# Kernel optimization log

Measured on AMD Instinct MI355X. Metric: run time of the kernel, lower is better.

Reference implementation:

```python
import jax, jax.numpy as jnp
import numpy as np
import math

STD = math.exp(0.0025)  # exp(0.5 * 0.005) from log_sigma = 0.005
C = 0.5 * math.log(2 * math.pi)
B, X, H, Z, L, W = 8192, 512, 256, 64, 16, 32

def _predict(h, Wd, bd, Wo, bo):
    return jax.nn.sigmoid(jax.nn.relu(h @ Wd.T + bd) @ Wo.T + bo)

def _gru(xin, h, Wih, Whh, bih, bhh):
    gi = xin @ Wih.T + bih
    gh = h @ Whh.T + bhh
    ir, iz, inn = jnp.split(gi, 3, axis=1)
    hr, hz, hn = jnp.split(gh, 3, axis=1)
    r = jax.nn.sigmoid(ir + hr)
    zt = jax.nn.sigmoid(iz + hz)
    n = jnp.tanh(inn + r * hn)
    return (1.0 - zt) * n + zt * h

def setup_inputs():
    key = jax.random.key(0)
    ks = iter(jax.random.split(key, 40))
    def nrm(shape, s=0.05):
        return jax.random.normal(next(ks), shape, dtype=jnp.float32) * s
    return {
        "x": jax.random.uniform(next(ks), (B, X), dtype=jnp.float32),
        "workers": jax.random.uniform(next(ks), (W, B, L), dtype=jnp.float32),
        "Wf1": nrm((H, X)), "bf1": jnp.zeros((H,)),
        "Wf2": nrm((1, H)), "bf2": jnp.zeros((1,)),
        "eWih": nrm((L, 3 * H, X + 1)), "eWhh": nrm((L, 3 * H, H)),
        "ebih": jnp.zeros((L, 3 * H)), "ebhh": jnp.zeros((L, 3 * H)),
        "eWd": nrm((L, H, H)), "ebd": jnp.zeros((L, H)),
        "eWo": nrm((L, 1, H)), "ebo": jnp.zeros((L, 1)),
        "Wmu": nrm((Z, H)), "bmu": jnp.zeros((Z,)),
        "Wlv": nrm((Z, H)), "blv": jnp.zeros((Z,)),
        "dWih": nrm((L, 3 * H, Z + 1)), "dWhh": nrm((L, 3 * H, H)),
        "dbih": jnp.zeros((L, 3 * H)), "dbhh": jnp.zeros((L, 3 * H)),
        "dWd": nrm((L, H, H)), "dbd": jnp.zeros((L, H)),
        "dWo": nrm((L, W, H)), "dbo": jnp.zeros((L, W)),
        "Wr": nrm((X, H)), "br": jnp.zeros((X,)),
        "enc_eps": jax.random.normal(next(ks), (L, B, H), dtype=jnp.float32),
        "samp_eps": jax.random.normal(next(ks), (B, Z), dtype=jnp.float32),
        "dec_eps": jax.random.uniform(next(ks), (L, B, H), dtype=jnp.float32),
    }

def _forward(x, workers, Wf1, bf1, Wf2, bf2, eWih, eWhh, ebih, ebhh, eWd, ebd, eWo, ebo,
             Wmu, bmu, Wlv, blv, dWih, dWhh, dbih, dbhh, dWd, dbd, dWo, dbo, Wr, br,
             enc_eps, samp_eps, dec_eps):
    nB = x.shape[0]
    h_dim = eWhh.shape[2]
    # Encoder: t[:,0] = firstcell(x)
    t0 = _predict(x, Wf1, bf1, Wf2, bf2)[:, 0]
    z0 = jnp.zeros((nB, h_dim), dtype=x.dtype)

    def enc_step(carry, xs):
        z, ti = carry
        Wih, Whh, bih, bhh, Wd, bd, Wo, bo, eps = xs
        tmp = (ti >= 0.5).astype(x.dtype)
        mu = _gru(jnp.concatenate([x, tmp[:, None]], axis=1), z, Wih, Whh, bih, bhh)
        znew = mu + STD * eps
        tn = _predict(znew, Wd, bd, Wo, bo)[:, 0]
        return (znew, tn), ti

    (z_fin, _), tcols = jax.lax.scan(
        enc_step, (z0, t0), (eWih, eWhh, ebih, ebhh, eWd, ebd, eWo, ebo, enc_eps))
    t = tcols.T  # [B, L]
    mu_z = z_fin @ Wmu.T + bmu
    log_var = jax.nn.softplus(z_fin @ Wlv.T + blv)
    latent = mu_z + jnp.exp(0.5 * log_var) * samp_eps
    tmp_t = (t > 0.5).astype(x.dtype)

    def dec_step(zt, xs):
        Wih, Whh, bih, bhh, Wd, bd, Wo, bo, tcol, eps = xs
        mu = _gru(jnp.concatenate([latent, tcol[:, None]], axis=1), zt, Wih, Whh, bih, bhh)
        znew = mu + STD * eps  # decoder uses uniform eps (torch.rand)
        return znew, _predict(znew, Wd, bd, Wo, bo)

    zT, preds = jax.lax.scan(
        dec_step, jnp.zeros((nB, h_dim), dtype=x.dtype),
        (dWih, dWhh, dbih, dbhh, dWd, dbd, dWo, dbo, tmp_t.T, dec_eps))
    worker_preds = jnp.transpose(preds, (2, 1, 0))  # [L,B,W] -> [W,B,L]
    recon = jax.nn.sigmoid(zT @ Wr.T + br)
    log_p_x = jnp.sum(x * jnp.log(recon), axis=1)
    logp = jnp.clip(jnp.log(worker_preds), -100.0)
    log1mp = jnp.clip(jnp.log1p(-worker_preds), -100.0)
    bce = -(workers * logp + (1.0 - workers) * log1mp)
    log_p_y = -jnp.sum(jnp.sum(bce, axis=0), axis=1)
    workers_bar = jnp.mean(workers, axis=0)
    log_kl = jnp.sum(t * (jnp.log(t + 1e-6) - jnp.log(workers_bar + 1e-6)), axis=1)
    log_p_z = jnp.sum(-C - latent ** 2 / 2, axis=-1)
    log_q = jnp.sum(-C - log_var / 2 - (latent - mu_z) ** 2 / (2 * jnp.exp(log_var)), axis=-1)
    loss = jnp.mean(log_q - log_p_z - log_p_y - log_p_x + log_kl)
    return t, loss

def reference(x, workers, Wf1, bf1, Wf2, bf2, eWih, eWhh, ebih, ebhh, eWd, ebd, eWo, ebo,
              Wmu, bmu, Wlv, blv, dWih, dWhh, dbih, dbhh, dWd, dbd, dWo, dbo, Wr, br,
              enc_eps, samp_eps, dec_eps):
    return _forward(x, workers, Wf1, bf1, Wf2, bf2, eWih, eWhh, ebih, ebhh, eWd, ebd,
                    eWo, ebo, Wmu, bmu, Wlv, blv, dWih, dWhh, dbih, dbhh, dWd, dbd,
                    dWo, dbo, Wr, br, enc_eps, samp_eps, dec_eps)
```

## Files before the change

### kernel.cpp

```cpp
#include <hip/hip_runtime.h>
#include <hip/hip_bf16.h>
#include <math.h>

#define B_ 8192
#define X_ 512
#define H_ 256
#define Z_ 64
#define L_ 16
#define W_ 32
#define G3_ 768

#define STDF 1.0025031276057952f
#define CC 0.9189385332046727f

typedef _Float16 f16x8 __attribute__((ext_vector_type(8)));
typedef float f32x4 __attribute__((ext_vector_type(4)));

__device__ __forceinline__ float sigm(float x) { return 1.0f / (1.0f + expf(-x)); }
__device__ __forceinline__ float logsig(float u) {
    return (u > 0.0f) ? -log1pf(expf(-u)) : (u - log1pf(expf(u)));
}

#define GLOAD16(gsrc, ldst) \
    __builtin_amdgcn_global_load_lds((const __attribute__((address_space(1))) unsigned int*)(gsrc), \
                                     (__attribute__((address_space(3))) unsigned int*)(ldst), 16, 0, 0)

#define WAITV(N) asm volatile("s_waitcnt vmcnt(" #N ")" ::: "memory")
#define SBAR()  do { __builtin_amdgcn_sched_barrier(0); __builtin_amdgcn_s_barrier(); } while (0)

template<int MODE, int KX, int FIRST>
__global__ __launch_bounds__(512) void gru_fused(
    const _Float16* __restrict__ A2,
    const _Float16* __restrict__ Wih,
    const float* __restrict__ bih,
    const _Float16* __restrict__ Whh,
    const float* __restrict__ bhh,
    const float* __restrict__ ec,
    const float* __restrict__ tcol,
    const float* __restrict__ eps,
    const _Float16* __restrict__ zh_in,
    float* __restrict__ z,
    _Float16* __restrict__ zh_out)
{
    constexpr int N1 = KX / 64;
    constexpr int NT = N1 + (FIRST ? 0 : 4);
    __shared__ char smem[2][(128 + 192) * 128];

    const int tid  = threadIdx.x;
    const int wave = tid >> 6;
    const int lane = tid & 63;
    const int wr   = wave >> 1;
    const int wc   = wave & 1;
    const int id   = blockIdx.x;
    const int xcd  = id & 7;
    const int wk   = id >> 3;
    const int bm   = (xcd * 8 + (wk >> 2)) * 128;
    const int h0   = (wk & 3) * 64;
    const int l15  = lane & 15;
    const int l4   = lane >> 4;

    f32x4 acc[2][6];
    f32x4 accN[2][2];
    #pragma unroll
    for (int a = 0; a < 2; ++a) {
        #pragma unroll
        for (int b = 0; b < 6; ++b) { f32x4 zz = {0.f,0.f,0.f,0.f}; acc[a][b] = zz; }
        #pragma unroll
        for (int b = 0; b < 2; ++b) { f32x4 zz = {0.f,0.f,0.f,0.f}; accN[a][b] = zz; }
    }

    auto stage = [&](int s, int pb) {
        char* As = smem[pb];
        char* Ws = smem[pb] + 128 * 128;
        const _Float16* srcA;
        const _Float16* srcW;
        int KA, k0;
        if (s < N1) { srcA = A2;    srcW = Wih; KA = KX;  k0 = s * 64; }
        else        { srcA = zh_in; srcW = Whh; KA = 256; k0 = (s - N1) * 64; }
        #pragma unroll
        for (int q = 0; q < 2; ++q) {
            int f   = q * 8192 + tid * 16;
            int row = f >> 7;
            int c   = ((f >> 4) & 7) ^ (row & 7);
            GLOAD16(srcA + (long)(bm + row) * KA + k0 + c * 8, As + f);
        }
        #pragma unroll
        for (int q = 0; q < 3; ++q) {
            int f   = q * 8192 + tid * 16;
            int rr  = f >> 7;
            int c   = ((f >> 4) & 7) ^ (rr & 7);
            int srow = (rr >> 6) * 256 + h0 + (rr & 63);
            GLOAD16(srcW + (long)srow * KA + k0 + c * 8, Ws + f);
        }
    };

    stage(0, 0);
    for (int s = 0; s < NT; ++s) {
        int pb = s & 1;
        if (s + 1 < NT) { stage(s + 1, pb ^ 1); WAITV(5); }
        else WAITV(0);
        SBAR();
        char* As = smem[pb];
        char* Ws = smem[pb] + 128 * 128;
        bool p1 = (s < N1);
        #pragma unroll
        for (int ks = 0; ks < 2; ++ks) {
            f16x8 af[2], bf[6];
            #pragma unroll
            for (int mi = 0; mi < 2; ++mi) {
                int row = wr * 32 + mi * 16 + l15;
                int c   = (ks * 4 + l4) ^ (row & 7);
                af[mi] = *(const f16x8*)(As + row * 128 + c * 16);
            }
            #pragma unroll
            for (int ni = 0; ni < 6; ++ni) {
                int rr = (ni >> 1) * 64 + wc * 32 + (ni & 1) * 16 + l15;
                int c  = (ks * 4 + l4) ^ (rr & 7);
                bf[ni] = *(const f16x8*)(Ws + rr * 128 + c * 16);
            }
            if (p1) {
                #pragma unroll
                for (int mi = 0; mi < 2; ++mi) {
                    #pragma unroll
                    for (int ni = 0; ni < 4; ++ni)
                        acc[mi][ni] = __builtin_amdgcn_mfma_f32_16x16x32_f16(
                            af[mi], bf[ni], acc[mi][ni], 0, 0, 0);
                    #pragma unroll
                    for (int ni = 4; ni < 6; ++ni)
                        accN[mi][ni - 4] = __builtin_amdgcn_mfma_f32_16x16x32_f16(
                            af[mi], bf[ni], accN[mi][ni - 4], 0, 0, 0);
                }
            } else {
                #pragma unroll
                for (int mi = 0; mi < 2; ++mi)
                    #pragma unroll
                    for (int ni = 0; ni < 6; ++ni)
                        acc[mi][ni] = __builtin_amdgcn_mfma_f32_16x16x32_f16(
                            af[mi], bf[ni], acc[mi][ni], 0, 0, 0);
            }
        }
        SBAR();
    }

    #pragma unroll
    for (int mi = 0; mi < 2; ++mi)
        #pragma unroll
        for (int r = 0; r < 4; ++r) {
            int grow = bm + wr * 32 + mi * 16 + l4 * 4 + r;
            float tv = tcol[(long)grow * L_];
            float ext = (MODE == 1) ? (tv >= 0.5f ? 1.0f : 0.0f)
                                    : (tv >  0.5f ? 1.0f : 0.0f);
            #pragma unroll
            for (int hb = 0; hb < 2; ++hb) {
                int h = h0 + wc * 32 + hb * 16 + l15;
                float rpre = acc[mi][hb][r]     + bih[h]       + bhh[h]       + ext * ec[h];
                float zpre = acc[mi][2 + hb][r] + bih[256 + h] + bhh[256 + h] + ext * ec[256 + h];
                float hn   = acc[mi][4 + hb][r] + bhh[512 + h];
                float in_  = accN[mi][hb][r]    + bih[512 + h] + ext * ec[512 + h];
                float rg = sigm(rpre);
                float zt = sigm(zpre);
                float n  = tanhf(in_ + rg * hn);
                long zi = (long)grow * 256 + h;
                float zold = FIRST ? 0.0f : z[zi];
                float v = (1.0f - zt) * n + zt * zold + STDF * eps[zi];
                z[zi] = v;
                zh_out[zi] = (_Float16)v;
            }
        }
}

__global__ __launch_bounds__(256) void predict_head512(
    const _Float16* __restrict__ A,
    const _Float16* __restrict__ Wd,
    const float* __restrict__ bd,
    const float* __restrict__ wo,
    const float* __restrict__ bo,
    float* __restrict__ out, int ostride)
{
    constexpr int K = 512;
    constexpr int NT = K / 64;
    __shared__ char smem[2][(32 + 256) * 128];
    __shared__ float part[32][4];

    const int tid  = threadIdx.x;
    const int wave = tid >> 6;
    const int lane = tid & 63;
    const int bm   = blockIdx.x * 32;
    const int l15  = lane & 15;
    const int l4   = lane >> 4;

    f32x4 acc[2][4];
    #pragma unroll
    for (int a = 0; a < 2; ++a)
        #pragma unroll
        for (int b = 0; b < 4; ++b) { f32x4 zz = {0.f,0.f,0.f,0.f}; acc[a][b] = zz; }

    auto stage = [&](int s, int pb) {
        char* As = smem[pb];
        char* Ws = smem[pb] + 32 * 128;
        int k0 = s * 64;
        {
            int o   = wave * 1024 + lane * 16;
            int row = o >> 7;
            int c   = ((o >> 4) & 7) ^ (row & 7);
            GLOAD16(A + (long)(bm + row) * K + k0 + c * 8, As + wave * 1024);
        }
        #pragma unroll
        for (int it = 0; it < 8; ++it) {
            int q   = it * 4 + wave;
            int o   = q * 1024 + lane * 16;
            int row = o >> 7;
            int c   = ((o >> 4) & 7) ^ (row & 7);
            GLOAD16(Wd + (long)row * K + k0 + c * 8, Ws + q * 1024);
        }
    };

    stage(0, 0);
    for (int s = 0; s < NT; ++s) {
        int pb = s & 1;
        if (s + 1 < NT) { stage(s + 1, pb ^ 1); WAITV(9); }
        else WAITV(0);
        SBAR();
        char* As = smem[pb];
        char* Ws = smem[pb] + 32 * 128;
        #pragma unroll
        for (int ks = 0; ks < 2; ++ks) {
            f16x8 af[2], bf[4];
            #pragma unroll
            for (int mi = 0; mi < 2; ++mi) {
                int row = mi * 16 + l15;
                int c   = (ks * 4 + l4) ^ (row & 7);
                af[mi] = *(const f16x8*)(As + row * 128 + c * 16);
            }
            #pragma unroll
            for (int ni = 0; ni < 4; ++ni) {
                int row = wave * 64 + ni * 16 + l15;
                int c   = (ks * 4 + l4) ^ (row & 7);
                bf[ni] = *(const f16x8*)(Ws + row * 128 + c * 16);
            }
            #pragma unroll
            for (int mi = 0; mi < 2; ++mi)
                #pragma unroll
                for (int ni = 0; ni < 4; ++ni)
                    acc[mi][ni] = __builtin_amdgcn_mfma_f32_16x16x32_f16(
                        af[mi], bf[ni], acc[mi][ni], 0, 0, 0);
        }
        SBAR();
    }

    float bdv[4], wov[4];
    #pragma unroll
    for (int ni = 0; ni < 4; ++ni) {
        int col = wave * 64 + ni * 16 + l15;
        bdv[ni] = bd[col];
        wov[ni] = wo[col];
    }
    #pragma unroll
    for (int mi = 0; mi < 2; ++mi)
        #pragma unroll
        for (int r = 0; r < 4; ++r) {
            float s = 0.0f;
            #pragma unroll
            for (int ni = 0; ni < 4; ++ni) {
                float v = fmaxf(acc[mi][ni][r] + bdv[ni], 0.0f);
                s = fmaf(v, wov[ni], s);
            }
            #pragma unroll
            for (int off = 1; off < 16; off <<= 1) s += __shfl_xor(s, off, 16);
            if (l15 == 0) part[mi * 16 + l4 * 4 + r][wave] = s;
        }
    __syncthreads();
    if (tid < 32) {
        float u = part[tid][0] + part[tid][1] + part[tid][2] + part[tid][3] + bo[0];
        out[(long)(bm + tid) * ostride] = sigm(u);
    }
}

__global__ __launch_bounds__(256) void predict_fast(
    const _Float16* __restrict__ A,
    const _Float16* __restrict__ Wd,
    const float* __restrict__ bd,
    const float* __restrict__ wo,
    const float* __restrict__ bo,
    float* __restrict__ out, int ostride)
{
    __shared__ char Wl[131072];
    __shared__ char Al[16384];
    __shared__ float part[32][4];

    const int tid  = threadIdx.x;
    const int wave = tid >> 6;
    const int lane = tid & 63;
    const int bm   = blockIdx.x * 32;
    const int l15  = lane & 15;
    const int l4   = lane >> 4;

    #pragma unroll
    for (int q = 0; q < 32; ++q) {
        int f   = q * 4096 + tid * 16;
        int kc  = f >> 15;
        int o   = f & 32767;
        int row = o >> 7;
        int c   = ((o >> 4) & 7) ^ (row & 7);
        GLOAD16(Wd + (long)row * 256 + kc * 64 + c * 8, Wl + f);
    }
    #pragma unroll
    for (int q = 0; q < 4; ++q) {
        int f   = q * 4096 + tid * 16;
        int kc  = f >> 12;
        int o   = f & 4095;
        int row = o >> 7;
        int c   = ((o >> 4) & 7) ^ (row & 7);
        GLOAD16(A + (long)(bm + row) * 256 + kc * 64 + c * 8, Al + f);
    }
    WAITV(0);
    __syncthreads();

    f32x4 acc[2][4];
    #pragma unroll
    for (int a = 0; a < 2; ++a)
        #pragma unroll
        for (int b = 0; b < 4; ++b) { f32x4 zz = {0.f,0.f,0.f,0.f}; acc[a][b] = zz; }

    #pragma unroll
    for (int kc = 0; kc < 4; ++kc)
        #pragma unroll
        for (int ks = 0; ks < 2; ++ks) {
            f16x8 af[2], bf[4];
            #pragma unroll
            for (int mi = 0; mi < 2; ++mi) {
                int row = mi * 16 + l15;
                int c   = (ks * 4 + l4) ^ (row & 7);
                af[mi] = *(const f16x8*)(Al + kc * 4096 + row * 128 + c * 16);
            }
            #pragma unroll
            for (int ni = 0; ni < 4; ++ni) {
                int row = wave * 64 + ni * 16 + l15;
                int c   = (ks * 4 + l4) ^ (row & 7);
                bf[ni] = *(const f16x8*)(Wl + kc * 32768 + row * 128 + c * 16);
            }
            #pragma unroll
            for (int mi = 0; mi < 2; ++mi)
                #pragma unroll
                for (int ni = 0; ni < 4; ++ni)
                    acc[mi][ni] = __builtin_amdgcn_mfma_f32_16x16x32_f16(
                        af[mi], bf[ni], acc[mi][ni], 0, 0, 0);
        }

    float bdv[4], wov[4];
    #pragma unroll
    for (int ni = 0; ni < 4; ++ni) {
        int col = wave * 64 + ni * 16 + l15;
        bdv[ni] = bd[col];
        wov[ni] = wo[col];
    }
    #pragma unroll
    for (int mi = 0; mi < 2; ++mi)
        #pragma unroll
        for (int r = 0; r < 4; ++r) {
            float s = 0.0f;
            #pragma unroll
            for (int ni = 0; ni < 4; ++ni) {
                float v = fmaxf(acc[mi][ni][r] + bdv[ni], 0.0f);
                s = fmaf(v, wov[ni], s);
            }
            #pragma unroll
            for (int off = 1; off < 16; off <<= 1) s += __shfl_xor(s, off, 16);
            if (l15 == 0) part[mi * 16 + l4 * 4 + r][wave] = s;
        }
    __syncthreads();
    if (tid < 32) {
        float u = part[tid][0] + part[tid][1] + part[tid][2] + part[tid][3] + bo[0];
        out[(long)(bm + tid) * ostride] = sigm(u);
    }
}

__global__ __launch_bounds__(256) void dec_head_bce_fast(
    const _Float16* __restrict__ A,
    const _Float16* __restrict__ Wd,
    const float* __restrict__ bd,
    const _Float16* __restrict__ Wo,
    const float* __restrict__ bo,
    const float* __restrict__ wt,
    float* __restrict__ bacc)
{
    __shared__ char Wl[131072];
    __shared__ _Float16 ds[32 * 264];
    __shared__ float part[32][2];

    const int tid  = threadIdx.x;
    const int wave = tid >> 6;
    const int lane = tid & 63;
    const int bm   = blockIdx.x * 32;
    const int l15  = lane & 15;
    const int l4   = lane >> 4;

    #pragma unroll
    for (int q = 0; q < 32; ++q) {
        int f   = q * 4096 + tid * 16;
        int kc  = f >> 15;
        int o   = f & 32767;
        int row = o >> 7;
        int c   = ((o >> 4) & 7) ^ (row & 7);
        GLOAD16(Wd + (long)row * 256 + kc * 64 + c * 8, Wl + f);
    }
    f16x8 afr[8];
    #pragma unroll
    for (int kc = 0; kc < 4; ++kc)
        #pragma unroll
        for (int mi = 0; mi < 2; ++mi) {
            int row = mi * 16 + l15;
            afr[kc * 2 + mi] = *(const f16x8*)(A + (long)(bm + row) * 256 + kc * 64 + l4 * 8);
        }

    f32x4 acc[2][4];
    #pragma unroll
    for (int a = 0; a < 2; ++a)
        #pragma unroll
        for (int b = 0; b < 4; ++b) { f32x4 zz = {0.f,0.f,0.f,0.f}; acc[a][b] = zz; }

    WAITV(0);
    __syncthreads();

    #pragma unroll
    for (int kc = 0; kc < 4; ++kc) {
        f16x8 bf[4];
        #pragma unroll
        for (int ni = 0; ni < 4; ++ni) {
            int row = wave * 64 + ni * 16 + l15;
            int c   = (0 * 4 + l4) ^ (row & 7);
            bf[ni] = *(const f16x8*)(Wl + kc * 32768 + row * 128 + c * 16);
        }
        #pragma unroll
        for (int mi = 0; mi < 2; ++mi)
            #pragma unroll
            for (int ni = 0; ni < 4; ++ni)
                acc[mi][ni] = __builtin_amdgcn_mfma_f32_16x16x32_f16(
                    afr[kc * 2 + mi], bf[ni], acc[mi][ni], 0, 0, 0);
    }
    #pragma unroll
    for (int kc = 0; kc < 4; ++kc)
        #pragma unroll
        for (int mi = 0; mi < 2; ++mi) {
            int row = mi * 16 + l15;
            afr[kc * 2 + mi] = *(const f16x8*)(A + (long)(bm + row) * 256 + kc * 64 + 32 + l4 * 8);
        }
    #pragma unroll
    for (int kc = 0; kc < 4; ++kc) {
        f16x8 bf[4];
        #pragma unroll
        for (int ni = 0; ni < 4; ++ni) {
            int row = wave * 64 + ni * 16 + l15;
            int c   = (1 * 4 + l4) ^ (row & 7);
            bf[ni] = *(const f16x8*)(Wl + kc * 32768 + row * 128 + c * 16);
        }
        #pragma unroll
        for (int mi = 0; mi < 2; ++mi)
            #pragma unroll
            for (int ni = 0; ni < 4; ++ni)
                acc[mi][ni] = __builtin_amdgcn_mfma_f32_16x16x32_f16(
                    afr[kc * 2 + mi], bf[ni], acc[mi][ni], 0, 0, 0);
    }

    #pragma unroll
    for (int mi = 0; mi < 2; ++mi)
        #pragma unroll
        for (int r = 0; r < 4; ++r) {
            int row = mi * 16 + l4 * 4 + r;
            #pragma unroll
            for (int ni = 0; ni < 4; ++ni) {
                int col = wave * 64 + ni * 16 + l15;
                ds[row * 264 + col] = (_Float16)fmaxf(acc[mi][ni][r] + bd[col], 0.0f);
            }
        }
    __syncthreads();

    const int rh = wave >> 1;
    const int ch = wave & 1;
    f32x4 acc2 = {0.f, 0.f, 0.f, 0.f};
    #pragma unroll
    for (int k = 0; k < 8; ++k) {
        f16x8 bf2 = *(const f16x8*)(Wo + (long)(ch * 16 + l15) * 256 + k * 32 + l4 * 8);
        f16x8 af  = *(const f16x8*)(ds + (rh * 16 + l15) * 264 + k * 32 + l4 * 8);
        acc2 = __builtin_amdgcn_mfma_f32_16x16x32_f16(af, bf2, acc2, 0, 0, 0);
    }

    #pragma unroll
    for (int r = 0; r < 4; ++r) {
        int row = rh * 16 + l4 * 4 + r;
        int w = ch * 16 + l15;
        float u = acc2[r] + bo[w];
        float logp   = fmaxf(logsig(u),  -100.0f);
        float log1mp = fmaxf(logsig(-u), -100.0f);
        float wk = wt[(long)(bm + row) * W_ + w];
        float s = -(wk * logp + (1.0f - wk) * log1mp);
        #pragma unroll
        for (int off = 1; off < 16; off <<= 1) s += __shfl_xor(s, off, 16);
        if (l15 == 0) part[row][ch] = s;
    }
    __syncthreads();
    if (tid < 32) bacc[bm + tid] += part[tid][0] + part[tid][1];
}

__global__ __launch_bounds__(256) void latent_fused(
    const _Float16* __restrict__ A,
    const _Float16* __restrict__ Wml,
    const float* __restrict__ bml,
    const float* __restrict__ seps,
    _Float16* __restrict__ lath,
    float* __restrict__ lq, float* __restrict__ lpz)
{
    __shared__ char Wl[65536];
    __shared__ char Al[16384];
    __shared__ float muv[32][129];

    const int tid  = threadIdx.x;
    const int wave = tid >> 6;
    const int lane = tid & 63;
    const int bm   = blockIdx.x * 32;
    const int l15  = lane & 15;
    const int l4   = lane >> 4;

    #pragma unroll
    for (int q = 0; q < 16; ++q) {
        int f   = q * 4096 + tid * 16;
        int kc  = f >> 14;
        int o   = f & 16383;
        int row = o >> 7;
        int c   = ((o >> 4) & 7) ^ (row & 7);
        GLOAD16(Wml + (long)row * 256 + kc * 64 + c * 8, Wl + f);
    }
    #pragma unroll
    for (int q = 0; q < 4; ++q) {
        int f   = q * 4096 + tid * 16;
        int kc  = f >> 12;
        int o   = f & 4095;
        int row = o >> 7;
        int c   = ((o >> 4) & 7) ^ (row & 7);
        GLOAD16(A + (long)(bm + row) * 256 + kc * 64 + c * 8, Al + f);
    }
    WAITV(0);
    __syncthreads();

    f32x4 acc[2][2];
    #pragma unroll
    for (int a = 0; a < 2; ++a)
        #pragma unroll
        for (int b = 0; b < 2; ++b) { f32x4 zz = {0.f,0.f,0.f,0.f}; acc[a][b] = zz; }

    #pragma unroll
    for (int kc = 0; kc < 4; ++kc)
        #pragma unroll
        for (int ks = 0; ks < 2; ++ks) {
            f16x8 af[2], bf[2];
            #pragma unroll
            for (int mi = 0; mi < 2; ++mi) {
                int row = mi * 16 + l15;
                int c   = (ks * 4 + l4) ^ (row & 7);
                af[mi] = *(const f16x8*)(Al + kc * 4096 + row * 128 + c * 16);
            }
            #pragma unroll
            for (int ni = 0; ni < 2; ++ni) {
                int row = wave * 32 + ni * 16 + l15;
                int c   = (ks * 4 + l4) ^ (row & 7);
                bf[ni] = *(const f16x8*)(Wl + kc * 16384 + row * 128 + c * 16);
            }
            #pragma unroll
            for (int mi = 0; mi < 2; ++mi)
                #pragma unroll
                for (int ni = 0; ni < 2; ++ni)
                    acc[mi][ni] = __builtin_amdgcn_mfma_f32_16x16x32_f16(
                        af[mi], bf[ni], acc[mi][ni], 0, 0, 0);
        }

    #pragma unroll
    for (int mi = 0; mi < 2; ++mi)
        #pragma unroll
        for (int r = 0; r < 4; ++r) {
            int row = mi * 16 + l4 * 4 + r;
            #pragma unroll
            for (int ni = 0; ni < 2; ++ni) {
                int col = wave * 32 + ni * 16 + l15;
                muv[row][col] = acc[mi][ni][r] + bml[col];
            }
        }
    __syncthreads();

    int rsub = lane >> 3;
    int row  = wave * 8 + rsub;
    int zlo  = lane & 7;
    float lpz_c = 0.0f, lq_c = 0.0f;
    #pragma unroll
    for (int j = 0; j < 8; ++j) {
        int zc = zlo * 8 + j;
        float mu = muv[row][zc];
        float sp = muv[row][64 + zc];
        float lv = (sp > 0.0f) ? (sp + log1pf(expf(-sp))) : log1pf(expf(sp));
        float e  = seps[(long)(bm + row) * Z_ + zc];
        float lat = mu + expf(0.5f * lv) * e;
        lath[(long)(bm + row) * Z_ + zc] = (_Float16)lat;
        lpz_c += -CC - 0.5f * lat * lat;
        float d = lat - mu;
        lq_c += -CC - 0.5f * lv - d * d / (2.0f * expf(lv));
    }
    #pragma unroll
    for (int off = 1; off < 8; off <<= 1) {
        lpz_c += __shfl_xor(lpz_c, off, 8);
        lq_c  += __shfl_xor(lq_c, off, 8);
    }
    if (zlo == 0) { lpz[bm + row] = lpz_c; lq[bm + row] = lq_c; }
}

__global__ __launch_bounds__(256) void recon_logpx_gemm(
    const _Float16* __restrict__ A,
    const _Float16* __restrict__ Wt,
    const float* __restrict__ bias,
    const float* __restrict__ x,
    float* __restrict__ lpx)
{
    constexpr int K = 256;
    constexpr int NT = 4;
    __shared__ char smem[2][(128 + 128) * 128];
    __shared__ float part[128][2];

    const int tid  = threadIdx.x;
    const int wave = tid >> 6;
    const int lane = tid & 63;
    const int wr   = wave >> 1;
    const int wc   = wave & 1;
    const int bm   = blockIdx.y * 128;
    const int bn   = blockIdx.x * 128;
    const int l15  = lane & 15;
    const int l4   = lane >> 4;

    f32x4 acc[4][4];
    #pragma unroll
    for (int a = 0; a < 4; ++a)
        #pragma unroll
        for (int b = 0; b < 4; ++b) { f32x4 zz = {0.f,0.f,0.f,0.f}; acc[a][b] = zz; }

    auto stage = [&](int s, int pb) {
        char* As = smem[pb];
        char* Ws = smem[pb] + 128 * 128;
        int k0 = s * 64;
        #pragma unroll
        for (int it = 0; it < 4; ++it) {
            int q   = it * 4 + wave;
            int o   = q * 1024 + lane * 16;
            int row = o >> 7;
            int c   = ((o >> 4) & 7) ^ (row & 7);
            GLOAD16(A + (long)(bm + row) * K + k0 + c * 8, As + q * 1024);
        }
        #pragma unroll
        for (int it = 0; it < 4; ++it) {
            int q   = it * 4 + wave;
            int o   = q * 1024 + lane * 16;
            int row = o >> 7;
            int c   = ((o >> 4) & 7) ^ (row & 7);
            GLOAD16(Wt + (long)(bn + row) * K + k0 + c * 8, Ws + q * 1024);
        }
    };

    stage(0, 0);
    for (int s = 0; s < NT; ++s) {
        int pb = s & 1;
        if (s + 1 < NT) { stage(s + 1, pb ^ 1); WAITV(8); }
        else WAITV(0);
        SBAR();
        char* As = smem[pb];
        char* Ws = smem[pb] + 128 * 128;
        #pragma unroll
        for (int ks = 0; ks < 2; ++ks) {
            f16x8 af[4], bf[4];
            #pragma unroll
            for (int mi = 0; mi < 4; ++mi) {
                int row = wr * 64 + mi * 16 + l15;
                int c   = (ks * 4 + l4) ^ (row & 7);
                af[mi] = *(const f16x8*)(As + row * 128 + c * 16);
            }
            #pragma unroll
            for (int ni = 0; ni < 4; ++ni) {
                int row = wc * 64 + ni * 16 + l15;
                int c   = (ks * 4 + l4) ^ (row & 7);
                bf[ni] = *(const f16x8*)(Ws + row * 128 + c * 16);
            }
            #pragma unroll
            for (int mi = 0; mi < 4; ++mi)
                #pragma unroll
                for (int ni = 0; ni < 4; ++ni)
                    acc[mi][ni] = __builtin_amdgcn_mfma_f32_16x16x32_f16(
                        af[mi], bf[ni], acc[mi][ni], 0, 0, 0);
        }
        SBAR();
    }

    #pragma unroll
    for (int mi = 0; mi < 4; ++mi)
        #pragma unroll
        for (int r = 0; r < 4; ++r) {
            int grow = bm + wr * 64 + mi * 16 + l4 * 4 + r;
            float s = 0.0f;
            #pragma unroll
            for (int ni = 0; ni < 4; ++ni) {
                int gcol = bn + wc * 64 + ni * 16 + l15;
                float u = acc[mi][ni][r] + bias[gcol];
                s = fmaf(x[(long)grow * X_ + gcol], logsig(u), s);
            }
            #pragma unroll
            for (int off = 1; off < 16; off <<= 1) s += __shfl_xor(s, off, 16);
            if (l15 == 0) part[wr * 64 + mi * 16 + l4 * 4 + r][wc] = s;
        }
    __syncthreads();
    if (tid < 128) atomicAdd(&lpx[bm + tid], part[tid][0] + part[tid][1]);
}

__global__ __launch_bounds__(256) void wtrans(
    const float* __restrict__ workers, float* __restrict__ wt,
    float* __restrict__ bacc, float* __restrict__ lpx)
{
    long idx = (long)blockIdx.x * 256 + threadIdx.x;
    int w = idx & 31;
    long b = idx >> 5;
    const float* src = workers + (w * (long)B_ + b) * L_;
    #pragma unroll
    for (int l = 0; l < L_; ++l)
        wt[((long)l * B_ + b) * W_ + w] = src[l];
    if (w == 0) { bacc[b] = 0.0f; lpx[b] = 0.0f; }
}

struct ConvJobs {
    const float* s[10];
    _Float16* d[10];
};
__device__ __constant__ const long CJ_CNT[10] = {
    (long)B_ * X_, (long)H_ * X_, (long)L_ * G3_ * H_, (long)L_ * H_ * H_,
    (long)L_ * G3_ * H_, (long)L_ * H_ * H_, (long)L_ * W_ * H_,
    (long)X_ * H_, (long)Z_ * H_, (long)Z_ * H_
};
#define CJ_TOTAL 13008896L

__global__ __launch_bounds__(256) void conv_multi(ConvJobs J)
{
    long i8 = ((long)blockIdx.x * 256 + threadIdx.x) * 8;
    if (i8 >= CJ_TOTAL) return;
    long rem = i8; int j = 0;
    #pragma unroll
    for (int k = 0; k < 9; ++k)
        if (rem >= CJ_CNT[k]) { rem -= CJ_CNT[k]; ++j; } else break;
    const float* s = J.s[j] + rem;
    f16x8 o;
    #pragma unroll
    for (int q = 0; q < 8; ++q) o[q] = (_Float16)s[q];
    *(f16x8*)(J.d[j] + rem) = o;
}

__global__ __launch_bounds__(256) void conv_f16(
    const float* __restrict__ src, _Float16* __restrict__ dst,
    int Ks, int Kd, long total)
{
    long i = ((long)blockIdx.x * 256 + threadIdx.x) * 8;
    if (i >= total) return;
    long r = i / Kd, k = i - r * Kd;
    const float* s = src + r * Ks + k;
    f16x8 o;
    #pragma unroll
    for (int j = 0; j < 8; ++j) o[j] = (_Float16)s[j];
    *(f16x8*)(dst + i) = o;
}

__global__ __launch_bounds__(256) void extract_col(
    const float* __restrict__ src, float* __restrict__ dst, int Ks, int col, int R)
{
    int i = blockIdx.x * 256 + threadIdx.x;
    if (i < R) dst[i] = src[(long)i * Ks + col];
}

__global__ void stack_bias(const float* __restrict__ a, const float* __restrict__ b,
                           float* __restrict__ o)
{
    int i = threadIdx.x;
    o[i] = (i < 64) ? a[i] : b[i - 64];
}

__global__ __launch_bounds__(256) void kl_kernel(
    const float* __restrict__ tmat, const float* __restrict__ workers,
    float* __restrict__ lkl)
{
    int b = blockIdx.x * 256 + threadIdx.x;
    float wb[L_];
    #pragma unroll
    for (int l = 0; l < L_; ++l) wb[l] = 0.0f;
    for (int w = 0; w < W_; ++w) {
        const float* p = workers + ((long)w * B_ + b) * L_;
        #pragma unroll
        for (int l = 0; l < L_; ++l) wb[l] += p[l];
    }
    float s = 0.0f;
    #pragma unroll
    for (int l = 0; l < L_; ++l) {
        float wbar = wb[l] * (1.0f / 32.0f);
        float tv = tmat[(long)b * L_ + l];
        s += tv * (logf(tv + 1e-6f) - logf(wbar + 1e-6f));
    }
    lkl[b] = s;
}

__global__ __launch_bounds__(1024) void final_reduce(
    const float* __restrict__ lq, const float* __restrict__ lpz,
    const float* __restrict__ bacc, const float* __restrict__ lpx,
    const float* __restrict__ lkl, float* __restrict__ out)
{
    __shared__ float red[16];
    float s = 0.0f;
    for (int b = threadIdx.x; b < B_; b += 1024)
        s += lq[b] - lpz[b] + bacc[b] - lpx[b] + lkl[b];
    #pragma unroll
    for (int off = 32; off; off >>= 1) s += __shfl_down(s, off);
    int wave = threadIdx.x >> 6, lane = threadIdx.x & 63;
    if (lane == 0) red[wave] = s;
    __syncthreads();
    if (threadIdx.x == 0) {
        float t = 0.0f;
        for (int i = 0; i < 16; ++i) t += red[i];
        out[0] = t / (float)B_;
    }
}

extern "C" void kernel_launch(void* const* d_in, const int* in_sizes, int n_in,
                              void* d_out, int out_size, void* d_ws, size_t ws_size,
                              hipStream_t stream)
{
    const float* x       = (const float*)d_in[0];
    const float* workers = (const float*)d_in[1];
    const float* Wf1     = (const float*)d_in[2];
    const float* bf1     = (const float*)d_in[3];
    const float* Wf2     = (const float*)d_in[4];
    const float* bf2     = (const float*)d_in[5];
    const float* eWih    = (const float*)d_in[6];
    const float* eWhh    = (const float*)d_in[7];
    const float* ebih    = (const float*)d_in[8];
    const float* ebhh    = (const float*)d_in[9];
    const float* eWd     = (const float*)d_in[10];
    const float* ebd     = (const float*)d_in[11];
    const float* eWo     = (const float*)d_in[12];
    const float* ebo     = (const float*)d_in[13];
    const float* Wmu     = (const float*)d_in[14];
    const float* bmu     = (const float*)d_in[15];
    const float* Wlv     = (const float*)d_in[16];
    const float* blv     = (const float*)d_in[17];
    const float* dWih    = (const float*)d_in[18];
    const float* dWhh    = (const float*)d_in[19];
    const float* dbih    = (const float*)d_in[20];
    const float* dbhh    = (const float*)d_in[21];
    const float* dWd     = (const float*)d_in[22];
    const float* dbd     = (const float*)d_in[23];
    const float* dWo     = (const float*)d_in[24];
    const float* dbo     = (const float*)d_in[25];
    const float* Wr      = (const float*)d_in[26];
    const float* br      = (const float*)d_in[27];
    const float* enc_eps = (const float*)d_in[28];
    const float* samp_eps= (const float*)d_in[29];
    const float* dec_eps = (const float*)d_in[30];

    float* t    = (float*)d_out;
    float* loss = t + (long)B_ * L_;

    char* p = (char*)d_ws;
    auto alloc = [&](size_t bytes) {
        char* r = p;
        p += (bytes + 255) & ~(size_t)255;
        return r;
    };
    _Float16* xh    = (_Float16*)alloc((size_t)B_ * X_ * 2);
    _Float16* zha   = (_Float16*)alloc((size_t)B_ * H_ * 2);
    _Float16* zhb   = (_Float16*)alloc((size_t)B_ * H_ * 2);
    _Float16* lath  = (_Float16*)alloc((size_t)B_ * Z_ * 2);
    _Float16* Wf1h  = (_Float16*)alloc((size_t)H_ * X_ * 2);
    _Float16* eWihh = (_Float16*)alloc((size_t)L_ * G3_ * X_ * 2);
    _Float16* eWhhh = (_Float16*)alloc((size_t)L_ * G3_ * H_ * 2);
    _Float16* eWdh  = (_Float16*)alloc((size_t)L_ * H_ * H_ * 2);
    _Float16* dWihh = (_Float16*)alloc((size_t)L_ * G3_ * Z_ * 2);
    _Float16* dWhhh = (_Float16*)alloc((size_t)L_ * G3_ * H_ * 2);
    _Float16* dWdh  = (_Float16*)alloc((size_t)L_ * H_ * H_ * 2);
    _Float16* dWoh  = (_Float16*)alloc((size_t)L_ * W_ * H_ * 2);
    _Float16* Wrh   = (_Float16*)alloc((size_t)X_ * H_ * 2);
    _Float16* Wmlh  = (_Float16*)alloc((size_t)128 * H_ * 2);
    float* bml    = (float*)alloc(128 * 4);
    float* eWihc  = (float*)alloc((size_t)L_ * G3_ * 4);
    float* dWihc  = (float*)alloc((size_t)L_ * G3_ * 4);
    float* z      = (float*)alloc((size_t)B_ * H_ * 4);
    float* wt     = (float*)alloc((size_t)L_ * B_ * W_ * 4);
    float* lq     = (float*)alloc((size_t)B_ * 4);
    float* lpz    = (float*)alloc((size_t)B_ * 4);
    float* lpx    = (float*)alloc((size_t)B_ * 4);
    float* lkl    = (float*)alloc((size_t)B_ * 4);
    float* bacc   = (float*)alloc((size_t)B_ * 4);

    const dim3 blk(256);
    const int nBH = B_ * H_;
    auto cgrid = [](long total) { return dim3((unsigned)((total / 8 + 255) / 256)); };

    ConvJobs J;
    J.s[0] = x;    J.d[0] = xh;
    J.s[1] = Wf1;  J.d[1] = Wf1h;
    J.s[2] = eWhh; J.d[2] = eWhhh;
    J.s[3] = eWd;  J.d[3] = eWdh;
    J.s[4] = dWhh; J.d[4] = dWhhh;
    J.s[5] = dWd;  J.d[5] = dWdh;
    J.s[6] = dWo;  J.d[6] = dWoh;
    J.s[7] = Wr;   J.d[7] = Wrh;
    J.s[8] = Wmu;  J.d[8] = Wmlh;
    J.s[9] = Wlv;  J.d[9] = Wmlh + (long)Z_ * H_;
    conv_multi<<<(CJ_TOTAL / 8 + 255) / 256, blk, 0, stream>>>(J);
    conv_f16<<<cgrid((long)L_ * G3_ * X_), blk, 0, stream>>>(eWih, eWihh, X_ + 1, X_, (long)L_ * G3_ * X_);
    conv_f16<<<cgrid((long)L_ * G3_ * Z_), blk, 0, stream>>>(dWih, dWihh, Z_ + 1, Z_, (long)L_ * G3_ * Z_);
    stack_bias<<<1, 128, 0, stream>>>(bmu, blv, bml);
    extract_col<<<(L_ * G3_ + 255) / 256, blk, 0, stream>>>(eWih, eWihc, X_ + 1, X_, L_ * G3_);
    extract_col<<<(L_ * G3_ + 255) / 256, blk, 0, stream>>>(dWih, dWihc, Z_ + 1, Z_, L_ * G3_);
    wtrans<<<(W_ * B_) / 256, blk, 0, stream>>>(workers, wt, bacc, lpx);

    predict_head512<<<B_ / 32, blk, 0, stream>>>(xh, Wf1h, bf1, Wf2, bf2, t, L_);

    _Float16* zcur = zha;
    _Float16* znxt = zhb;
    for (int l = 0; l < L_; ++l) {
        if (l == 0)
            gru_fused<1, X_, 1><<<256, 512, 0, stream>>>(
                xh, eWihh, ebih, eWhhh, ebhh, eWihc, t, enc_eps, zcur, z, znxt);
        else
            gru_fused<1, X_, 0><<<256, 512, 0, stream>>>(
                xh, eWihh + (long)l * G3_ * X_, ebih + (long)l * G3_,
                eWhhh + (long)l * G3_ * H_, ebhh + (long)l * G3_,
                eWihc + (long)l * G3_, t + l, enc_eps + (long)l * nBH,
                zcur, z, znxt);
        _Float16* tmp = zcur; zcur = znxt; znxt = tmp;
        if (l < L_ - 1)
            predict_fast<<<B_ / 32, blk, 0, stream>>>(
                zcur, eWdh + (long)l * H_ * H_, ebd + (long)l * H_,
                eWo + (long)l * H_, ebo + l, t + (l + 1), L_);
    }

    latent_fused<<<B_ / 32, blk, 0, stream>>>(zcur, Wmlh, bml, samp_eps, lath, lq, lpz);

    zcur = zha; znxt = zhb;
    for (int l = 0; l < L_; ++l) {
        if (l == 0)
            gru_fused<2, Z_, 1><<<256, 512, 0, stream>>>(
                lath, dWihh, dbih, dWhhh, dbhh, dWihc, t, dec_eps, zcur, z, znxt);
        else
            gru_fused<2, Z_, 0><<<256, 512, 0, stream>>>(
                lath, dWihh + (long)l * G3_ * Z_, dbih + (long)l * G3_,
                dWhhh + (long)l * G3_ * H_, dbhh + (long)l * G3_,
                dWihc + (long)l * G3_, t + l, dec_eps + (long)l * nBH,
                zcur, z, znxt);
        _Float16* tmp = zcur; zcur = znxt; znxt = tmp;
        dec_head_bce_fast<<<B_ / 32, blk, 0, stream>>>(
            zcur, dWdh + (long)l * H_ * H_, dbd + (long)l * H_,
            dWoh + (long)l * W_ * H_, dbo + (long)l * W_,
            wt + (long)l * B_ * W_, bacc);
    }

    recon_logpx_gemm<<<dim3(X_ / 128, B_ / 128), blk, 0, stream>>>(
        zcur, Wrh, br, x, lpx);
    kl_kernel<<<B_ / 256, blk, 0, stream>>>(t, workers, lkl);
    final_reduce<<<1, 1024, 0, stream>>>(lq, lpz, bacc, lpx, lkl, loss);
}
```

Measured before the change: 1.074 ms.

## Fuse predict and decoder heads into GRU step kernels; merge prep launches

```diff
diff --git a/kernel.cpp b/kernel.cpp
--- a/kernel.cpp
+++ b/kernel.cpp
@@ -26,10 +26,13 @@
                                      (__attribute__((address_space(3))) unsigned int*)(ldst), 16, 0, 0)
 
 #define WAITV(N) asm volatile("s_waitcnt vmcnt(" #N ")" ::: "memory")
+#define WAITV0() asm volatile("s_waitcnt vmcnt(0)" ::: "memory")
 #define SBAR()  do { __builtin_amdgcn_sched_barrier(0); __builtin_amdgcn_s_barrier(); } while (0)
 
-template<int MODE, int KX, int FIRST>
-__global__ __launch_bounds__(512) void gru_fused(
+#define MFMA16(a, b, c) __builtin_amdgcn_mfma_f32_16x16x32_f16((a), (b), (c), 0, 0, 0)
+
+template<int FIRST>
+__global__ __launch_bounds__(512, 4) void enc_gru(
     const _Float16* __restrict__ A2,
     const _Float16* __restrict__ Wih,
     const float* __restrict__ bih,
@@ -37,14 +40,21 @@
     const float* __restrict__ bhh,
     const float* __restrict__ ec,
     const float* __restrict__ tcol,
+    const _Float16* __restrict__ Wdp,
+    const float* __restrict__ bdp,
+    const float* __restrict__ wop,
+    const float* __restrict__ bop,
+    float* __restrict__ tout,
     const float* __restrict__ eps,
     const _Float16* __restrict__ zh_in,
     float* __restrict__ z,
     _Float16* __restrict__ zh_out)
 {
+    constexpr int KX = 512;
     constexpr int N1 = KX / 64;
-    constexpr int NT = N1 + (FIRST ? 0 : 4);
-    __shared__ char smem[2][(128 + 192) * 128];
+    constexpr int NT = FIRST ? N1 : (N1 + 4);
+    __shared__ char smem[2][40960];
+    __shared__ float uarr[128];
 
     const int tid  = threadIdx.x;
     const int wave = tid >> 6;
@@ -59,6 +69,83 @@
     const int l15  = lane & 15;
     const int l4   = lane >> 4;
 
+    if (!FIRST) {
+        float up0 = 0.f, up1 = 0.f, up2 = 0.f, up3 = 0.f;
+        for (int ch = 0; ch < 2; ++ch) {
+            f32x4 acc2[8];
+            #pragma unroll
+            for (int i = 0; i < 8; ++i) { f32x4 zz = {0.f,0.f,0.f,0.f}; acc2[i] = zz; }
+            auto pstage = [&](int s, int pb) {
+                char* As = smem[pb];
+                char* Ws = smem[pb] + 16384;
+                int k0 = s * 64;
+                #pragma unroll
+                for (int q = 0; q < 2; ++q) {
+                    int f = q * 8192 + tid * 16;
+                    int row = f >> 7;
+                    int c = ((f >> 4) & 7) ^ (row & 7);
+                    GLOAD16(zh_in + (long)(bm + row) * 256 + k0 + c * 8, As + f);
+                }
+                #pragma unroll
+                for (int q = 0; q < 2; ++q) {
+                    int f = q * 8192 + tid * 16;
+                    int row = f >> 7;
+                    int c = ((f >> 4) & 7) ^ (row & 7);
+                    GLOAD16(Wdp + (long)(ch * 128 + row) * 256 + k0 + c * 8, Ws + f);
+                }
+            };
+            pstage(0, 0);
+            for (int s = 0; s < 4; ++s) {
+                int pb = s & 1;
+                if (s + 1 < 4) { pstage(s + 1, pb ^ 1); WAITV(4); }
+                else WAITV0();
+                SBAR();
+                char* As = smem[pb];
+                char* Ws = smem[pb] + 16384;
+                #pragma unroll
+                for (int ks = 0; ks < 2; ++ks) {
+                    int arow = wave * 16 + l15;
+                    int ca = (ks * 4 + l4) ^ (arow & 7);
+                    f16x8 af = *(const f16x8*)(As + arow * 128 + ca * 16);
+                    #pragma unroll
+                    for (int ni = 0; ni < 8; ++ni) {
+                        int wrow = ni * 16 + l15;
+                        int cw = (ks * 4 + l4) ^ (wrow & 7);
+                        f16x8 bf = *(const f16x8*)(Ws + wrow * 128 + cw * 16);
+                        acc2[ni] = MFMA16(af, bf, acc2[ni]);
+                    }
+                }
+                SBAR();
+            }
+            #pragma unroll
+            for (int ni = 0; ni < 8; ++ni) {
+                int col = ch * 128 + ni * 16 + l15;
+                float bdv = bdp[col], wov = wop[col];
+                up0 = fmaf(fmaxf(acc2[ni][0] + bdv, 0.f), wov, up0);
+                up1 = fmaf(fmaxf(acc2[ni][1] + bdv, 0.f), wov, up1);
+                up2 = fmaf(fmaxf(acc2[ni][2] + bdv, 0.f), wov, up2);
+                up3 = fmaf(fmaxf(acc2[ni][3] + bdv, 0.f), wov, up3);
+            }
+        }
+        #pragma unroll
+        for (int off = 1; off < 16; off <<= 1) {
+            up0 += __shfl_xor(up0, off, 16);
+            up1 += __shfl_xor(up1, off, 16);
+            up2 += __shfl_xor(up2, off, 16);
+            up3 += __shfl_xor(up3, off, 16);
+        }
+        if (l15 == 0) {
+            float b0 = bop[0];
+            uarr[wave * 16 + l4 * 4 + 0] = up0 + b0;
+            uarr[wave * 16 + l4 * 4 + 1] = up1 + b0;
+            uarr[wave * 16 + l4 * 4 + 2] = up2 + b0;
+            uarr[wave * 16 + l4 * 4 + 3] = up3 + b0;
+        }
+        __syncthreads();
+        if (h0 == 0 && tid < 128)
+            tout[(long)(bm + tid) * L_] = sigm(uarr[tid]);
+    }
+
     f32x4 acc[2][6];
     f32x4 accN[2][2];
     #pragma unroll
@@ -71,7 +158,7 @@
 
     auto stage = [&](int s, int pb) {
         char* As = smem[pb];
-        char* Ws = smem[pb] + 128 * 128;
+        char* Ws = smem[pb] + 16384;
         const _Float16* srcA;
         const _Float16* srcW;
         int KA, k0;
@@ -98,10 +185,10 @@
     for (int s = 0; s < NT; ++s) {
         int pb = s & 1;
         if (s + 1 < NT) { stage(s + 1, pb ^ 1); WAITV(5); }
-        else WAITV(0);
+        else WAITV0();
         SBAR();
         char* As = smem[pb];
-        char* Ws = smem[pb] + 128 * 128;
+        char* Ws = smem[pb] + 16384;
         bool p1 = (s < N1);
         #pragma unroll
         for (int ks = 0; ks < 2; ++ks) {
@@ -123,20 +210,17 @@
                 for (int mi = 0; mi < 2; ++mi) {
                     #pragma unroll
                     for (int ni = 0; ni < 4; ++ni)
-                        acc[mi][ni] = __builtin_amdgcn_mfma_f32_16x16x32_f16(
-                            af[mi], bf[ni], acc[mi][ni], 0, 0, 0);
+                        acc[mi][ni] = MFMA16(af[mi], bf[ni], acc[mi][ni]);
                     #pragma unroll
                     for (int ni = 4; ni < 6; ++ni)
-                        accN[mi][ni - 4] = __builtin_amdgcn_mfma_f32_16x16x32_f16(
-                            af[mi], bf[ni], accN[mi][ni - 4], 0, 0, 0);
+                        accN[mi][ni - 4] = MFMA16(af[mi], bf[ni], accN[mi][ni - 4]);
                 }
             } else {
                 #pragma unroll
                 for (int mi = 0; mi < 2; ++mi)
                     #pragma unroll
                     for (int ni = 0; ni < 6; ++ni)
-                        acc[mi][ni] = __builtin_amdgcn_mfma_f32_16x16x32_f16(
-                            af[mi], bf[ni], acc[mi][ni], 0, 0, 0);
+                        acc[mi][ni] = MFMA16(af[mi], bf[ni], acc[mi][ni]);
             }
         }
         SBAR();
@@ -146,10 +230,15 @@
     for (int mi = 0; mi < 2; ++mi)
         #pragma unroll
         for (int r = 0; r < 4; ++r) {
-            int grow = bm + wr * 32 + mi * 16 + l4 * 4 + r;
-            float tv = tcol[(long)grow * L_];
-            float ext = (MODE == 1) ? (tv >= 0.5f ? 1.0f : 0.0f)
-                                    : (tv >  0.5f ? 1.0f : 0.0f);
+            int lrow = wr * 32 + mi * 16 + l4 * 4 + r;
+            int grow = bm + lrow;
+            float ext;
+            if (FIRST) {
+                float tv = tcol[(long)grow * L_];
+                ext = (tv >= 0.5f) ? 1.0f : 0.0f;
+            } else {
+                ext = (uarr[lrow] >= 0.0f) ? 1.0f : 0.0f;
+            }
             #pragma unroll
             for (int hb = 0; hb < 2; ++hb) {
                 int h = h0 + wc * 32 + hb * 16 + l15;
@@ -169,6 +258,410 @@
         }
 }
 
+__device__ void dec_gru_role(char (*smem)[40960],
+    const _Float16* __restrict__ A2, const _Float16* __restrict__ Wih,
+    const float* __restrict__ bih, const _Float16* __restrict__ Whh,
+    const float* __restrict__ bhh, const float* __restrict__ ec,
+    const float* __restrict__ tcol, const float* __restrict__ eps,
+    const _Float16* __restrict__ zh_in, float* __restrict__ z,
+    _Float16* __restrict__ zh_out, bool first)
+{
+    constexpr int KX = Z_;
+    constexpr int N1 = 1;
+    const int NT = first ? 1 : 5;
+
+    const int tid  = threadIdx.x;
+    const int wave = tid >> 6;
+    const int lane = tid & 63;
+    const int wr   = wave >> 1;
+    const int wc   = wave & 1;
+    const int id   = blockIdx.x;
+    const int xcd  = id & 7;
+    const int wk   = id >> 3;
+    const int bm   = (xcd * 8 + (wk >> 2)) * 128;
+    const int h0   = (wk & 3) * 64;
+    const int l15  = lane & 15;
+    const int l4   = lane >> 4;
+
+    f32x4 acc[2][6];
+    f32x4 accN[2][2];
+    #pragma unroll
+    for (int a = 0; a < 2; ++a) {
+        #pragma unroll
+        for (int b = 0; b < 6; ++b) { f32x4 zz = {0.f,0.f,0.f,0.f}; acc[a][b] = zz; }
+        #pragma unroll
+        for (int b = 0; b < 2; ++b) { f32x4 zz = {0.f,0.f,0.f,0.f}; accN[a][b] = zz; }
+    }
+
+    auto stage = [&](int s, int pb) {
+        char* As = smem[pb];
+        char* Ws = smem[pb] + 16384;
+        const _Float16* srcA;
+        const _Float16* srcW;
+        int KA, k0;
+        if (s < N1) { srcA = A2;    srcW = Wih; KA = KX;  k0 = s * 64; }
+        else        { srcA = zh_in; srcW = Whh; KA = 256; k0 = (s - N1) * 64; }
+        #pragma unroll
+        for (int q = 0; q < 2; ++q) {
+            int f   = q * 8192 + tid * 16;
+            int row = f >> 7;
+            int c   = ((f >> 4) & 7) ^ (row & 7);
+            GLOAD16(srcA + (long)(bm + row) * KA + k0 + c * 8, As + f);
+        }
+        #pragma unroll
+        for (int q = 0; q < 3; ++q) {
+            int f   = q * 8192 + tid * 16;
+            int rr  = f >> 7;
+            int c   = ((f >> 4) & 7) ^ (rr & 7);
+            int srow = (rr >> 6) * 256 + h0 + (rr & 63);
+            GLOAD16(srcW + (long)srow * KA + k0 + c * 8, Ws + f);
+        }
+    };
+
+    stage(0, 0);
+    for (int s = 0; s < NT; ++s) {
+        int pb = s & 1;
+        if (s + 1 < NT) { stage(s + 1, pb ^ 1); WAITV(5); }
+        else WAITV0();
+        SBAR();
+        char* As = smem[pb];
+        char* Ws = smem[pb] + 16384;
+        bool p1 = (s < N1);
+        #pragma unroll
+        for (int ks = 0; ks < 2; ++ks) {
+            f16x8 af[2], bf[6];
+            #pragma unroll
+            for (int mi = 0; mi < 2; ++mi) {
+                int row = wr * 32 + mi * 16 + l15;
+                int c   = (ks * 4 + l4) ^ (row & 7);
+                af[mi] = *(const f16x8*)(As + row * 128 + c * 16);
+            }
+            #pragma unroll
+            for (int ni = 0; ni < 6; ++ni) {
+                int rr = (ni >> 1) * 64 + wc * 32 + (ni & 1) * 16 + l15;
+                int c  = (ks * 4 + l4) ^ (rr & 7);
+                bf[ni] = *(const f16x8*)(Ws + rr * 128 + c * 16);
+            }
+            if (p1) {
+                #pragma unroll
+                for (int mi = 0; mi < 2; ++mi) {
+                    #pragma unroll
+                    for (int ni = 0; ni < 4; ++ni)
+                        acc[mi][ni] = MFMA16(af[mi], bf[ni], acc[mi][ni]);
+                    #pragma unroll
+                    for (int ni = 4; ni < 6; ++ni)
+                        accN[mi][ni - 4] = MFMA16(af[mi], bf[ni], accN[mi][ni - 4]);
+                }
+            } else {
+                #pragma unroll
+                for (int mi = 0; mi < 2; ++mi)
+                    #pragma unroll
+                    for (int ni = 0; ni < 6; ++ni)
+                        acc[mi][ni] = MFMA16(af[mi], bf[ni], acc[mi][ni]);
+            }
+        }
+        SBAR();
+    }
+
+    #pragma unroll
+    for (int mi = 0; mi < 2; ++mi)
+        #pragma unroll
+        for (int r = 0; r < 4; ++r) {
+            int grow = bm + wr * 32 + mi * 16 + l4 * 4 + r;
+            float tv = tcol[(long)grow * L_];
+            float ext = (tv > 0.5f) ? 1.0f : 0.0f;
+            #pragma unroll
+            for (int hb = 0; hb < 2; ++hb) {
+                int h = h0 + wc * 32 + hb * 16 + l15;
+                float rpre = acc[mi][hb][r]     + bih[h]       + bhh[h]       + ext * ec[h];
+                float zpre = acc[mi][2 + hb][r] + bih[256 + h] + bhh[256 + h] + ext * ec[256 + h];
+                float hn   = acc[mi][4 + hb][r] + bhh[512 + h];
+                float in_  = accN[mi][hb][r]    + bih[512 + h] + ext * ec[512 + h];
+                float rg = sigm(rpre);
+                float zt = sigm(zpre);
+                float n  = tanhf(in_ + rg * hn);
+                long zi = (long)grow * 256 + h;
+                float zold = first ? 0.0f : z[zi];
+                float v = (1.0f - zt) * n + zt * zold + STDF * eps[zi];
+                z[zi] = v;
+                zh_out[zi] = (_Float16)v;
+            }
+        }
+}
+
+__device__ void bce_role(char (*smem)[40960], float* auxp, int localblk,
+    const _Float16* __restrict__ A, const _Float16* __restrict__ Wd,
+    const float* __restrict__ bd, const _Float16* __restrict__ Wo,
+    const float* __restrict__ bo, const float* __restrict__ wtl,
+    float* __restrict__ bacc)
+{
+    const int tid  = threadIdx.x;
+    const bool act = tid < 256;
+    const int wave = tid >> 6;
+    const int lane = tid & 63;
+    const int bm2  = localblk * 32;
+    const int l15  = lane & 15;
+    const int l4   = lane >> 4;
+
+    f32x4 acc[2][2];
+    #pragma unroll
+    for (int a = 0; a < 2; ++a)
+        #pragma unroll
+        for (int b = 0; b < 2; ++b) { f32x4 zz = {0.f,0.f,0.f,0.f}; acc[a][b] = zz; }
+
+    auto stage = [&](int s, int pb) {
+        if (!act) return;
+        char* As = smem[pb];
+        char* Ws = smem[pb] + 4096;
+        int k0 = s * 64;
+        {
+            int f   = tid * 16;
+            int row = f >> 7;
+            int c   = ((f >> 4) & 7) ^ (row & 7);
+            GLOAD16(A + (long)(bm2 + row) * 256 + k0 + c * 8, As + f);
+        }
+        #pragma unroll
+        for (int q = 0; q < 8; ++q) {
+            int f   = q * 4096 + tid * 16;
+            int row = f >> 7;
+            int c   = ((f >> 4) & 7) ^ (row & 7);
+            GLOAD16(Wd + (long)row * 256 + k0 + c * 8, Ws + f);
+        }
+    };
+
+    stage(0, 0);
+    for (int s = 0; s < 4; ++s) {
+        int pb = s & 1;
+        if (s + 1 < 4) { stage(s + 1, pb ^ 1); WAITV(9); }
+        else WAITV0();
+        SBAR();
+        if (act) {
+            char* As = smem[pb];
+            char* Ws = smem[pb] + 4096;
+            #pragma unroll
+            for (int ks = 0; ks < 2; ++ks) {
+                f16x8 af[2], bf[2];
+                #pragma unroll
+                for (int mi = 0; mi < 2; ++mi) {
+                    int row = mi * 16 + l15;
+                    int c   = (ks * 4 + l4) ^ (row & 7);
+                    af[mi] = *(const f16x8*)(As + row * 128 + c * 16);
+                }
+                #pragma unroll
+                for (int ni = 0; ni < 2; ++ni) {
+                    int row = wave * 64 + ni * 16 + l15;
+                    int c   = (ks * 4 + l4) ^ (row & 7);
+                    bf[ni] = *(const f16x8*)(Ws + row * 128 + c * 16);
+                }
+                #pragma unroll
+                for (int mi = 0; mi < 2; ++mi)
+                    #pragma unroll
+                    for (int ni = 0; ni < 2; ++ni)
+                        acc[mi][ni] = MFMA16(af[mi], bf[ni], acc[mi][ni]);
+            }
+        }
+        SBAR();
+    }
+
+    _Float16* ds = (_Float16*)smem[0];
+    if (act) {
+        #pragma unroll
+        for (int mi = 0; mi < 2; ++mi)
+            #pragma unroll
+            for (int r = 0; r < 4; ++r) {
+                int row = mi * 16 + l4 * 4 + r;
+                #pragma unroll
+                for (int ni = 0; ni < 2; ++ni) {
+                    int col = wave * 64 + ni * 16 + l15;
+                    ds[row * 264 + col] = (_Float16)fmaxf(acc[mi][ni][r] + bd[col], 0.0f);
+                }
+            }
+    }
+    __syncthreads();
+
+    if (act) {
+        const int rh = wave >> 1;
+        const int ch = wave & 1;
+        f32x4 acc2 = {0.f, 0.f, 0.f, 0.f};
+        #pragma unroll
+        for (int k = 0; k < 8; ++k) {
+            f16x8 bf2 = *(const f16x8*)(Wo + (long)(ch * 16 + l15) * 256 + k * 32 + l4 * 8);
+            f16x8 af  = *(const f16x8*)(ds + (rh * 16 + l15) * 264 + k * 32 + l4 * 8);
+            acc2 = MFMA16(af, bf2, acc2);
+        }
+        #pragma unroll
+        for (int r = 0; r < 4; ++r) {
+            int row = rh * 16 + l4 * 4 + r;
+            int w = ch * 16 + l15;
+            float u = acc2[r] + bo[w];
+            float logp   = fmaxf(logsig(u),  -100.0f);
+            float log1mp = fmaxf(logsig(-u), -100.0f);
+            float wk = wtl[(long)(bm2 + row) * W_ + w];
+            float s = -(wk * logp + (1.0f - wk) * log1mp);
+            #pragma unroll
+            for (int off = 1; off < 16; off <<= 1) s += __shfl_xor(s, off, 16);
+            if (l15 == 0) auxp[row * 2 + ch] = s;
+        }
+    }
+    __syncthreads();
+    if (tid < 32) bacc[bm2 + tid] += auxp[tid * 2 + 0] + auxp[tid * 2 + 1];
+}
+
+__device__ void recon_role(char (*smem)[40960], float* auxp, int localblk,
+    const _Float16* __restrict__ A, const _Float16* __restrict__ Wt,
+    const float* __restrict__ bias, const float* __restrict__ x,
+    float* __restrict__ lpx)
+{
+    const int tid  = threadIdx.x;
+    const bool act = tid < 256;
+    const int wave = tid >> 6;
+    const int lane = tid & 63;
+    const int wr   = wave >> 1;
+    const int wc   = wave & 1;
+    const int bm   = (localblk >> 2) * 128;
+    const int bn   = (localblk & 3) * 128;
+    const int l15  = lane & 15;
+    const int l4   = lane >> 4;
+
+    f32x4 acc[4][4];
+    #pragma unroll
+    for (int a = 0; a < 4; ++a)
+        #pragma unroll
+        for (int b = 0; b < 4; ++b) { f32x4 zz = {0.f,0.f,0.f,0.f}; acc[a][b] = zz; }
+
+    auto stage = [&](int s, int pb) {
+        if (!act) return;
+        char* As = smem[pb];
+        char* Ws = smem[pb] + 16384;
+        int k0 = s * 64;
+        #pragma unroll
+        for (int it = 0; it < 4; ++it) {
+            int q   = it * 4 + wave;
+            int o   = q * 1024 + lane * 16;
+            int row = o >> 7;
+            int c   = ((o >> 4) & 7) ^ (row & 7);
+            GLOAD16(A + (long)(bm + row) * 256 + k0 + c * 8, As + q * 1024);
+        }
+        #pragma unroll
+        for (int it = 0; it < 4; ++it) {
+            int q   = it * 4 + wave;
+            int o   = q * 1024 + lane * 16;
+            int row = o >> 7;
+            int c   = ((o >> 4) & 7) ^ (row & 7);
+            GLOAD16(Wt + (long)(bn + row) * 256 + k0 + c * 8, Ws + q * 1024);
+        }
+    };
+
+    stage(0, 0);
+    for (int s = 0; s < 4; ++s) {
+        int pb = s & 1;
+        if (s + 1 < 4) { stage(s + 1, pb ^ 1); WAITV(8); }
+        else WAITV0();
+        SBAR();
+        if (act) {
+            char* As = smem[pb];
+            char* Ws = smem[pb] + 16384;
+            #pragma unroll
+            for (int ks = 0; ks < 2; ++ks) {
+                f16x8 af[4], bf[4];
+                #pragma unroll
+                for (int mi = 0; mi < 4; ++mi) {
+                    int row = wr * 64 + mi * 16 + l15;
+                    int c   = (ks * 4 + l4) ^ (row & 7);
+                    af[mi] = *(const f16x8*)(As + row * 128 + c * 16);
+                }
+                #pragma unroll
+                for (int ni = 0; ni < 4; ++ni) {
+                    int row = wc * 64 + ni * 16 + l15;
+                    int c   = (ks * 4 + l4) ^ (row & 7);
+                    bf[ni] = *(const f16x8*)(Ws + row * 128 + c * 16);
+                }
+                #pragma unroll
+                for (int mi = 0; mi < 4; ++mi)
+                    #pragma unroll
+                    for (int ni = 0; ni < 4; ++ni)
+                        acc[mi][ni] = MFMA16(af[mi], bf[ni], acc[mi][ni]);
+            }
+        }
+        SBAR();
+    }
+
+    if (act) {
+        #pragma unroll
+        for (int mi = 0; mi < 4; ++mi)
+            #pragma unroll
+            for (int r = 0; r < 4; ++r) {
+                int grow = bm + wr * 64 + mi * 16 + l4 * 4 + r;
+                float s = 0.0f;
+                #pragma unroll
+                for (int ni = 0; ni < 4; ++ni) {
+                    int gcol = bn + wc * 64 + ni * 16 + l15;
+                    float u = acc[mi][ni][r] + bias[gcol];
+                    s = fmaf(x[(long)grow * X_ + gcol], logsig(u), s);
+                }
+                #pragma unroll
+                for (int off = 1; off < 16; off <<= 1) s += __shfl_xor(s, off, 16);
+                if (l15 == 0) auxp[(wr * 64 + mi * 16 + l4 * 4 + r) * 2 + wc] = s;
+            }
+    }
+    __syncthreads();
+    if (tid < 128) atomicAdd(&lpx[bm + tid], auxp[tid * 2] + auxp[tid * 2 + 1]);
+}
+
+template<int FIRSTL>
+__global__ __launch_bounds__(512, 4) void dec_step(
+    const _Float16* lath, const _Float16* Wih, const float* bih,
+    const _Float16* Whh, const float* bhh, const float* ec,
+    const float* tcol, const float* eps,
+    const _Float16* zh_in, float* z, _Float16* zh_out,
+    const _Float16* WdB, const float* bdB, const _Float16* WoB,
+    const float* boB, const float* wtB, float* bacc,
+    const float* tmat, const float* workers, float* lkl)
+{
+    __shared__ char smem[2][40960];
+    __shared__ float auxp[256];
+
+    if (blockIdx.x < 256) {
+        dec_gru_role(smem, lath, Wih, bih, Whh, bhh, ec, tcol, eps,
+                     zh_in, z, zh_out, FIRSTL != 0);
+    } else if (FIRSTL) {
+        if (threadIdx.x < 256) {
+            int b = (blockIdx.x - 256) * 256 + threadIdx.x;
+            float wb[L_];
+            #pragma unroll
+            for (int l = 0; l < L_; ++l) wb[l] = 0.0f;
+            for (int w = 0; w < W_; ++w) {
+                const float* pw = workers + (w * (long)B_ + b) * L_;
+                #pragma unroll
+                for (int l = 0; l < L_; ++l) wb[l] += pw[l];
+            }
+            float s = 0.0f;
+            #pragma unroll
+            for (int l = 0; l < L_; ++l) {
+                float wbar = wb[l] * (1.0f / 32.0f);
+                float tv = tmat[(long)b * L_ + l];
+                s += tv * (logf(tv + 1e-6f) - logf(wbar + 1e-6f));
+            }
+            lkl[b] = s;
+        }
+    } else {
+        bce_role(smem, auxp, blockIdx.x - 256, zh_in, WdB, bdB, WoB, boB, wtB, bacc);
+    }
+}
+
+__global__ __launch_bounds__(512, 4) void dec_tail(
+    const _Float16* zh, const _Float16* WdB, const float* bdB,
+    const _Float16* WoB, const float* boB, const float* wtB, float* bacc,
+    const _Float16* Wrh, const float* br, const float* x, float* lpx)
+{
+    __shared__ char smem[2][40960];
+    __shared__ float auxp[256];
+    if (blockIdx.x < 256)
+        bce_role(smem, auxp, blockIdx.x, zh, WdB, bdB, WoB, boB, wtB, bacc);
+    else
+        recon_role(smem, auxp, blockIdx.x - 256, zh, Wrh, br, x, lpx);
+}
+
 __global__ __launch_bounds__(256) void predict_head512(
     const _Float16* __restrict__ A,
     const _Float16* __restrict__ Wd,
@@ -219,7 +712,7 @@
     for (int s = 0; s < NT; ++s) {
         int pb = s & 1;
         if (s + 1 < NT) { stage(s + 1, pb ^ 1); WAITV(9); }
-        else WAITV(0);
+        else WAITV0();
         SBAR();
         char* As = smem[pb];
         char* Ws = smem[pb] + 32 * 128;
@@ -242,8 +735,7 @@
             for (int mi = 0; mi < 2; ++mi)
                 #pragma unroll
                 for (int ni = 0; ni < 4; ++ni)
-                    acc[mi][ni] = __builtin_amdgcn_mfma_f32_16x16x32_f16(
-                        af[mi], bf[ni], acc[mi][ni], 0, 0, 0);
+                    acc[mi][ni] = MFMA16(af[mi], bf[ni], acc[mi][ni]);
         }
         SBAR();
     }
@@ -274,232 +766,6 @@
         float u = part[tid][0] + part[tid][1] + part[tid][2] + part[tid][3] + bo[0];
         out[(long)(bm + tid) * ostride] = sigm(u);
     }
-}
-
-__global__ __launch_bounds__(256) void predict_fast(
-    const _Float16* __restrict__ A,
-    const _Float16* __restrict__ Wd,
-    const float* __restrict__ bd,
-    const float* __restrict__ wo,
-    const float* __restrict__ bo,
-    float* __restrict__ out, int ostride)
-{
-    __shared__ char Wl[131072];
-    __shared__ char Al[16384];
-    __shared__ float part[32][4];
-
-    const int tid  = threadIdx.x;
-    const int wave = tid >> 6;
-    const int lane = tid & 63;
-    const int bm   = blockIdx.x * 32;
-    const int l15  = lane & 15;
-    const int l4   = lane >> 4;
-
-    #pragma unroll
-    for (int q = 0; q < 32; ++q) {
-        int f   = q * 4096 + tid * 16;
-        int kc  = f >> 15;
-        int o   = f & 32767;
-        int row = o >> 7;
-        int c   = ((o >> 4) & 7) ^ (row & 7);
-        GLOAD16(Wd + (long)row * 256 + kc * 64 + c * 8, Wl + f);
-    }
-    #pragma unroll
-    for (int q = 0; q < 4; ++q) {
-        int f   = q * 4096 + tid * 16;
-        int kc  = f >> 12;
-        int o   = f & 4095;
-        int row = o >> 7;
-        int c   = ((o >> 4) & 7) ^ (row & 7);
-        GLOAD16(A + (long)(bm + row) * 256 + kc * 64 + c * 8, Al + f);
-    }
-    WAITV(0);
-    __syncthreads();
-
-    f32x4 acc[2][4];
-    #pragma unroll
-    for (int a = 0; a < 2; ++a)
-        #pragma unroll
-        for (int b = 0; b < 4; ++b) { f32x4 zz = {0.f,0.f,0.f,0.f}; acc[a][b] = zz; }
-
-    #pragma unroll
-    for (int kc = 0; kc < 4; ++kc)
-        #pragma unroll
-        for (int ks = 0; ks < 2; ++ks) {
-            f16x8 af[2], bf[4];
-            #pragma unroll
-            for (int mi = 0; mi < 2; ++mi) {
-                int row = mi * 16 + l15;
-                int c   = (ks * 4 + l4) ^ (row & 7);
-                af[mi] = *(const f16x8*)(Al + kc * 4096 + row * 128 + c * 16);
-            }
-            #pragma unroll
-            for (int ni = 0; ni < 4; ++ni) {
-                int row = wave * 64 + ni * 16 + l15;
-                int c   = (ks * 4 + l4) ^ (row & 7);
-                bf[ni] = *(const f16x8*)(Wl + kc * 32768 + row * 128 + c * 16);
-            }
-            #pragma unroll
-            for (int mi = 0; mi < 2; ++mi)
-                #pragma unroll
-                for (int ni = 0; ni < 4; ++ni)
-                    acc[mi][ni] = __builtin_amdgcn_mfma_f32_16x16x32_f16(
-                        af[mi], bf[ni], acc[mi][ni], 0, 0, 0);
-        }
-
-    float bdv[4], wov[4];
-    #pragma unroll
-    for (int ni = 0; ni < 4; ++ni) {
-        int col = wave * 64 + ni * 16 + l15;
-        bdv[ni] = bd[col];
-        wov[ni] = wo[col];
-    }
-    #pragma unroll
-    for (int mi = 0; mi < 2; ++mi)
-        #pragma unroll
-        for (int r = 0; r < 4; ++r) {
-            float s = 0.0f;
-            #pragma unroll
-            for (int ni = 0; ni < 4; ++ni) {
-                float v = fmaxf(acc[mi][ni][r] + bdv[ni], 0.0f);
-                s = fmaf(v, wov[ni], s);
-            }
-            #pragma unroll
-            for (int off = 1; off < 16; off <<= 1) s += __shfl_xor(s, off, 16);
-            if (l15 == 0) part[mi * 16 + l4 * 4 + r][wave] = s;
-        }
-    __syncthreads();
-    if (tid < 32) {
-        float u = part[tid][0] + part[tid][1] + part[tid][2] + part[tid][3] + bo[0];
-        out[(long)(bm + tid) * ostride] = sigm(u);
-    }
-}
-
-__global__ __launch_bounds__(256) void dec_head_bce_fast(
-    const _Float16* __restrict__ A,
-    const _Float16* __restrict__ Wd,
-    const float* __restrict__ bd,
-    const _Float16* __restrict__ Wo,
-    const float* __restrict__ bo,
-    const float* __restrict__ wt,
-    float* __restrict__ bacc)
-{
-    __shared__ char Wl[131072];
-    __shared__ _Float16 ds[32 * 264];
-    __shared__ float part[32][2];
-
-    const int tid  = threadIdx.x;
-    const int wave = tid >> 6;
-    const int lane = tid & 63;
-    const int bm   = blockIdx.x * 32;
-    const int l15  = lane & 15;
-    const int l4   = lane >> 4;
-
-    #pragma unroll
-    for (int q = 0; q < 32; ++q) {
-        int f   = q * 4096 + tid * 16;
-        int kc  = f >> 15;
-        int o   = f & 32767;
-        int row = o >> 7;
-        int c   = ((o >> 4) & 7) ^ (row & 7);
-        GLOAD16(Wd + (long)row * 256 + kc * 64 + c * 8, Wl + f);
-    }
-    f16x8 afr[8];
-    #pragma unroll
-    for (int kc = 0; kc < 4; ++kc)
-        #pragma unroll
-        for (int mi = 0; mi < 2; ++mi) {
-            int row = mi * 16 + l15;
-            afr[kc * 2 + mi] = *(const f16x8*)(A + (long)(bm + row) * 256 + kc * 64 + l4 * 8);
-        }
-
-    f32x4 acc[2][4];
-    #pragma unroll
-    for (int a = 0; a < 2; ++a)
-        #pragma unroll
-        for (int b = 0; b < 4; ++b) { f32x4 zz = {0.f,0.f,0.f,0.f}; acc[a][b] = zz; }
-
-    WAITV(0);
-    __syncthreads();
-
-    #pragma unroll
-    for (int kc = 0; kc < 4; ++kc) {
-        f16x8 bf[4];
-        #pragma unroll
-        for (int ni = 0; ni < 4; ++ni) {
-            int row = wave * 64 + ni * 16 + l15;
-            int c   = (0 * 4 + l4) ^ (row & 7);
-            bf[ni] = *(const f16x8*)(Wl + kc * 32768 + row * 128 + c * 16);
-        }
-        #pragma unroll
-        for (int mi = 0; mi < 2; ++mi)
-            #pragma unroll
-            for (int ni = 0; ni < 4; ++ni)
-                acc[mi][ni] = __builtin_amdgcn_mfma_f32_16x16x32_f16(
-                    afr[kc * 2 + mi], bf[ni], acc[mi][ni], 0, 0, 0);
-    }
-    #pragma unroll
-    for (int kc = 0; kc < 4; ++kc)
-        #pragma unroll
-        for (int mi = 0; mi < 2; ++mi) {
-            int row = mi * 16 + l15;
-            afr[kc * 2 + mi] = *(const f16x8*)(A + (long)(bm + row) * 256 + kc * 64 + 32 + l4 * 8);
-        }
-    #pragma unroll
-    for (int kc = 0; kc < 4; ++kc) {
-        f16x8 bf[4];
-        #pragma unroll
-        for (int ni = 0; ni < 4; ++ni) {
-            int row = wave * 64 + ni * 16 + l15;
-            int c   = (1 * 4 + l4) ^ (row & 7);
-            bf[ni] = *(const f16x8*)(Wl + kc * 32768 + row * 128 + c * 16);
-        }
-        #pragma unroll
-        for (int mi = 0; mi < 2; ++mi)
-            #pragma unroll
-            for (int ni = 0; ni < 4; ++ni)
-                acc[mi][ni] = __builtin_amdgcn_mfma_f32_16x16x32_f16(
-                    afr[kc * 2 + mi], bf[ni], acc[mi][ni], 0, 0, 0);
-    }
-
-    #pragma unroll
-    for (int mi = 0; mi < 2; ++mi)
-        #pragma unroll
-        for (int r = 0; r < 4; ++r) {
-            int row = mi * 16 + l4 * 4 + r;
-            #pragma unroll
-            for (int ni = 0; ni < 4; ++ni) {
-                int col = wave * 64 + ni * 16 + l15;
-                ds[row * 264 + col] = (_Float16)fmaxf(acc[mi][ni][r] + bd[col], 0.0f);
-            }
-        }
-    __syncthreads();
-
-    const int rh = wave >> 1;
-    const int ch = wave & 1;
-    f32x4 acc2 = {0.f, 0.f, 0.f, 0.f};
-    #pragma unroll
-    for (int k = 0; k < 8; ++k) {
-        f16x8 bf2 = *(const f16x8*)(Wo + (long)(ch * 16 + l15) * 256 + k * 32 + l4 * 8);
-        f16x8 af  = *(const f16x8*)(ds + (rh * 16 + l15) * 264 + k * 32 + l4 * 8);
-        acc2 = __builtin_amdgcn_mfma_f32_16x16x32_f16(af, bf2, acc2, 0, 0, 0);
-    }
-
-    #pragma unroll
-    for (int r = 0; r < 4; ++r) {
-        int row = rh * 16 + l4 * 4 + r;
-        int w = ch * 16 + l15;
-        float u = acc2[r] + bo[w];
-        float logp   = fmaxf(logsig(u),  -100.0f);
-        float log1mp = fmaxf(logsig(-u), -100.0f);
-        float wk = wt[(long)(bm + row) * W_ + w];
-        float s = -(wk * logp + (1.0f - wk) * log1mp);
-        #pragma unroll
-        for (int off = 1; off < 16; off <<= 1) s += __shfl_xor(s, off, 16);
-        if (l15 == 0) part[row][ch] = s;
-    }
-    __syncthreads();
-    if (tid < 32) bacc[bm + tid] += part[tid][0] + part[tid][1];
 }
 
 __global__ __launch_bounds__(256) void latent_fused(
@@ -539,7 +805,7 @@
         int c   = ((o >> 4) & 7) ^ (row & 7);
         GLOAD16(A + (long)(bm + row) * 256 + kc * 64 + c * 8, Al + f);
     }
-    WAITV(0);
+    WAITV0();
     __syncthreads();
 
     f32x4 acc[2][2];
@@ -569,8 +835,7 @@
             for (int mi = 0; mi < 2; ++mi)
                 #pragma unroll
                 for (int ni = 0; ni < 2; ++ni)
-                    acc[mi][ni] = __builtin_amdgcn_mfma_f32_16x16x32_f16(
-                        af[mi], bf[ni], acc[mi][ni], 0, 0, 0);
+                    acc[mi][ni] = MFMA16(af[mi], bf[ni], acc[mi][ni]);
         }
 
     #pragma unroll
@@ -611,123 +876,6 @@
     if (zlo == 0) { lpz[bm + row] = lpz_c; lq[bm + row] = lq_c; }
 }
 
-__global__ __launch_bounds__(256) void recon_logpx_gemm(
-    const _Float16* __restrict__ A,
-    const _Float16* __restrict__ Wt,
-    const float* __restrict__ bias,
-    const float* __restrict__ x,
-    float* __restrict__ lpx)
-{
-    constexpr int K = 256;
-    constexpr int NT = 4;
-    __shared__ char smem[2][(128 + 128) * 128];
-    __shared__ float part[128][2];
-
-    const int tid  = threadIdx.x;
-    const int wave = tid >> 6;
-    const int lane = tid & 63;
-    const int wr   = wave >> 1;
-    const int wc   = wave & 1;
-    const int bm   = blockIdx.y * 128;
-    const int bn   = blockIdx.x * 128;
-    const int l15  = lane & 15;
-    const int l4   = lane >> 4;
-
-    f32x4 acc[4][4];
-    #pragma unroll
-    for (int a = 0; a < 4; ++a)
-        #pragma unroll
-        for (int b = 0; b < 4; ++b) { f32x4 zz = {0.f,0.f,0.f,0.f}; acc[a][b] = zz; }
-
-    auto stage = [&](int s, int pb) {
-        char* As = smem[pb];
-        char* Ws = smem[pb] + 128 * 128;
-        int k0 = s * 64;
-        #pragma unroll
-        for (int it = 0; it < 4; ++it) {
-            int q   = it * 4 + wave;
-            int o   = q * 1024 + lane * 16;
-            int row = o >> 7;
-            int c   = ((o >> 4) & 7) ^ (row & 7);
-            GLOAD16(A + (long)(bm + row) * K + k0 + c * 8, As + q * 1024);
-        }
-        #pragma unroll
-        for (int it = 0; it < 4; ++it) {
-            int q   = it * 4 + wave;
-            int o   = q * 1024 + lane * 16;
-            int row = o >> 7;
-            int c   = ((o >> 4) & 7) ^ (row & 7);
-            GLOAD16(Wt + (long)(bn + row) * K + k0 + c * 8, Ws + q * 1024);
-        }
-    };
-
-    stage(0, 0);
-    for (int s = 0; s < NT; ++s) {
-        int pb = s & 1;
-        if (s + 1 < NT) { stage(s + 1, pb ^ 1); WAITV(8); }
-        else WAITV(0);
-        SBAR();
-        char* As = smem[pb];
-        char* Ws = smem[pb] + 128 * 128;
-        #pragma unroll
-        for (int ks = 0; ks < 2; ++ks) {
-            f16x8 af[4], bf[4];
-            #pragma unroll
-            for (int mi = 0; mi < 4; ++mi) {
-                int row = wr * 64 + mi * 16 + l15;
-                int c   = (ks * 4 + l4) ^ (row & 7);
-                af[mi] = *(const f16x8*)(As + row * 128 + c * 16);
-            }
-            #pragma unroll
-            for (int ni = 0; ni < 4; ++ni) {
-                int row = wc * 64 + ni * 16 + l15;
-                int c   = (ks * 4 + l4) ^ (row & 7);
-                bf[ni] = *(const f16x8*)(Ws + row * 128 + c * 16);
-            }
-            #pragma unroll
-            for (int mi = 0; mi < 4; ++mi)
-                #pragma unroll
-                for (int ni = 0; ni < 4; ++ni)
-                    acc[mi][ni] = __builtin_amdgcn_mfma_f32_16x16x32_f16(
-                        af[mi], bf[ni], acc[mi][ni], 0, 0, 0);
-        }
-        SBAR();
-    }
-
-    #pragma unroll
-    for (int mi = 0; mi < 4; ++mi)
-        #pragma unroll
-        for (int r = 0; r < 4; ++r) {
-            int grow = bm + wr * 64 + mi * 16 + l4 * 4 + r;
-            float s = 0.0f;
-            #pragma unroll
-            for (int ni = 0; ni < 4; ++ni) {
-                int gcol = bn + wc * 64 + ni * 16 + l15;
-                float u = acc[mi][ni][r] + bias[gcol];
-                s = fmaf(x[(long)grow * X_ + gcol], logsig(u), s);
-            }
-            #pragma unroll
-            for (int off = 1; off < 16; off <<= 1) s += __shfl_xor(s, off, 16);
-            if (l15 == 0) part[wr * 64 + mi * 16 + l4 * 4 + r][wc] = s;
-        }
-    __syncthreads();
-    if (tid < 128) atomicAdd(&lpx[bm + tid], part[tid][0] + part[tid][1]);
-}
-
-__global__ __launch_bounds__(256) void wtrans(
-    const float* __restrict__ workers, float* __restrict__ wt,
-    float* __restrict__ bacc, float* __restrict__ lpx)
-{
-    long idx = (long)blockIdx.x * 256 + threadIdx.x;
-    int w = idx & 31;
-    long b = idx >> 5;
-    const float* src = workers + (w * (long)B_ + b) * L_;
-    #pragma unroll
-    for (int l = 0; l < L_; ++l)
-        wt[((long)l * B_ + b) * W_ + w] = src[l];
-    if (w == 0) { bacc[b] = 0.0f; lpx[b] = 0.0f; }
-}
-
 struct ConvJobs {
     const float* s[10];
     _Float16* d[10];
@@ -754,55 +902,51 @@
     *(f16x8*)(J.d[j] + rem) = o;
 }
 
-__global__ __launch_bounds__(256) void conv_f16(
-    const float* __restrict__ src, _Float16* __restrict__ dst,
-    int Ks, int Kd, long total)
+__global__ __launch_bounds__(256) void prep_misc(
+    const float* __restrict__ eWih, _Float16* __restrict__ eWihh,
+    const float* __restrict__ dWih, _Float16* __restrict__ dWihh,
+    const float* __restrict__ workers, float* __restrict__ wt,
+    float* __restrict__ bacc, float* __restrict__ lpx,
+    float* __restrict__ eWihc, float* __restrict__ dWihc,
+    const float* __restrict__ bmu, const float* __restrict__ blv,
+    float* __restrict__ bml)
 {
-    long i = ((long)blockIdx.x * 256 + threadIdx.x) * 8;
-    if (i >= total) return;
-    long r = i / Kd, k = i - r * Kd;
-    const float* s = src + r * Ks + k;
-    f16x8 o;
-    #pragma unroll
-    for (int j = 0; j < 8; ++j) o[j] = (_Float16)s[j];
-    *(f16x8*)(dst + i) = o;
-}
-
-__global__ __launch_bounds__(256) void extract_col(
-    const float* __restrict__ src, float* __restrict__ dst, int Ks, int col, int R)
-{
-    int i = blockIdx.x * 256 + threadIdx.x;
-    if (i < R) dst[i] = src[(long)i * Ks + col];
-}
-
-__global__ void stack_bias(const float* __restrict__ a, const float* __restrict__ b,
-                           float* __restrict__ o)
-{
-    int i = threadIdx.x;
-    o[i] = (i < 64) ? a[i] : b[i - 64];
-}
-
-__global__ __launch_bounds__(256) void kl_kernel(
-    const float* __restrict__ tmat, const float* __restrict__ workers,
-    float* __restrict__ lkl)
-{
-    int b = blockIdx.x * 256 + threadIdx.x;
-    float wb[L_];
-    #pragma unroll
-    for (int l = 0; l < L_; ++l) wb[l] = 0.0f;
-    for (int w = 0; w < W_; ++w) {
-        const float* p = workers + ((long)w * B_ + b) * L_;
-        #pragma unroll
-        for (int l = 0; l < L_; ++l) wb[l] += p[l];
-    }
-    float s = 0.0f;
-    #pragma unroll
-    for (int l = 0; l < L_; ++l) {
-        float wbar = wb[l] * (1.0f / 32.0f);
-        float tv = tmat[(long)b * L_ + l];
-        s += tv * (logf(tv + 1e-6f) - logf(wbar + 1e-6f));
-    }
-    lkl[b] = s;
+    int blk = blockIdx.x;
+    int tid = threadIdx.x;
+    if (blk < 3072) {
+        long i = ((long)blk * 256 + tid) * 8;
+        long r = i >> 9, k = i & 511;
+        const float* s = eWih + r * 513 + k;
+        f16x8 o;
+        #pragma unroll
+        for (int q = 0; q < 8; ++q) o[q] = (_Float16)s[q];
+        *(f16x8*)(eWihh + i) = o;
+    } else if (blk < 3456) {
+        long i = ((long)(blk - 3072) * 256 + tid) * 8;
+        long r = i >> 6, k = i & 63;
+        const float* s = dWih + r * 65 + k;
+        f16x8 o;
+        #pragma unroll
+        for (int q = 0; q < 8; ++q) o[q] = (_Float16)s[q];
+        *(f16x8*)(dWihh + i) = o;
+    } else if (blk < 4480) {
+        long idx = (long)(blk - 3456) * 256 + tid;
+        int w = idx & 31;
+        long b = idx >> 5;
+        const float* src = workers + (w * (long)B_ + b) * L_;
+        #pragma unroll
+        for (int l = 0; l < L_; ++l)
+            wt[((long)l * B_ + b) * W_ + w] = src[l];
+        if (w == 0) { bacc[b] = 0.0f; lpx[b] = 0.0f; }
+    } else if (blk < 4528) {
+        int i = (blk - 4480) * 256 + tid;
+        if (i < L_ * G3_) eWihc[i] = eWih[(long)i * 513 + 512];
+    } else if (blk < 4576) {
+        int i = (blk - 4528) * 256 + tid;
+        if (i < L_ * G3_) dWihc[i] = dWih[(long)i * 65 + 64];
+    } else {
+        if (tid < 128) bml[tid] = (tid < 64) ? bmu[tid] : blv[tid - 64];
+    }
 }
 
 __global__ __launch_bounds__(1024) void final_reduce(
@@ -872,8 +1016,8 @@
         return r;
     };
     _Float16* xh    = (_Float16*)alloc((size_t)B_ * X_ * 2);
-    _Float16* zha   = (_Float16*)alloc((size_t)B_ * H_ * 2);
-    _Float16* zhb   = (_Float16*)alloc((size_t)B_ * H_ * 2);
+    _Float16* zb0   = (_Float16*)alloc((size_t)B_ * H_ * 2);
+    _Float16* zb1   = (_Float16*)alloc((size_t)B_ * H_ * 2);
     _Float16* lath  = (_Float16*)alloc((size_t)B_ * Z_ * 2);
     _Float16* Wf1h  = (_Float16*)alloc((size_t)H_ * X_ * 2);
     _Float16* eWihh = (_Float16*)alloc((size_t)L_ * G3_ * X_ * 2);
@@ -898,7 +1042,6 @@
 
     const dim3 blk(256);
     const int nBH = B_ * H_;
-    auto cgrid = [](long total) { return dim3((unsigned)((total / 8 + 255) / 256)); };
 
     ConvJobs J;
     J.s[0] = x;    J.d[0] = xh;
@@ -912,56 +1055,57 @@
     J.s[8] = Wmu;  J.d[8] = Wmlh;
     J.s[9] = Wlv;  J.d[9] = Wmlh + (long)Z_ * H_;
     conv_multi<<<(CJ_TOTAL / 8 + 255) / 256, blk, 0, stream>>>(J);
-    conv_f16<<<cgrid((long)L_ * G3_ * X_), blk, 0, stream>>>(eWih, eWihh, X_ + 1, X_, (long)L_ * G3_ * X_);
-    conv_f16<<<cgrid((long)L_ * G3_ * Z_), blk, 0, stream>>>(dWih, dWihh, Z_ + 1, Z_, (long)L_ * G3_ * Z_);
-    stack_bias<<<1, 128, 0, stream>>>(bmu, blv, bml);
-    extract_col<<<(L_ * G3_ + 255) / 256, blk, 0, stream>>>(eWih, eWihc, X_ + 1, X_, L_ * G3_);
-    extract_col<<<(L_ * G3_ + 255) / 256, blk, 0, stream>>>(dWih, dWihc, Z_ + 1, Z_, L_ * G3_);
-    wtrans<<<(W_ * B_) / 256, blk, 0, stream>>>(workers, wt, bacc, lpx);
+    prep_misc<<<4577, blk, 0, stream>>>(eWih, eWihh, dWih, dWihh, workers, wt,
+                                        bacc, lpx, eWihc, dWihc, bmu, blv, bml);
 
     predict_head512<<<B_ / 32, blk, 0, stream>>>(xh, Wf1h, bf1, Wf2, bf2, t, L_);
 
-    _Float16* zcur = zha;
-    _Float16* znxt = zhb;
+    _Float16* zcur = zb0;
+    _Float16* znxt = zb1;
     for (int l = 0; l < L_; ++l) {
         if (l == 0)
-            gru_fused<1, X_, 1><<<256, 512, 0, stream>>>(
-                xh, eWihh, ebih, eWhhh, ebhh, eWihc, t, enc_eps, zcur, z, znxt);
+            enc_gru<1><<<256, 512, 0, stream>>>(
+                xh, eWihh, ebih, eWhhh, ebhh, eWihc, t,
+                nullptr, nullptr, nullptr, nullptr, nullptr,
+                enc_eps, zcur, z, znxt);
         else
-            gru_fused<1, X_, 0><<<256, 512, 0, stream>>>(
+            enc_gru<0><<<256, 512, 0, stream>>>(
                 xh, eWihh + (long)l * G3_ * X_, ebih + (long)l * G3_,
                 eWhhh + (long)l * G3_ * H_, ebhh + (long)l * G3_,
-                eWihc + (long)l * G3_, t + l, enc_eps + (long)l * nBH,
-                zcur, z, znxt);
+                eWihc + (long)l * G3_, nullptr,
+                eWdh + (long)(l - 1) * H_ * H_, ebd + (long)(l - 1) * H_,
+                eWo + (long)(l - 1) * H_, ebo + (l - 1), t + l,
+                enc_eps + (long)l * nBH, zcur, z, znxt);
         _Float16* tmp = zcur; zcur = znxt; znxt = tmp;
-        if (l < L_ - 1)
-            predict_fast<<<B_ / 32, blk, 0, stream>>>(
-                zcur, eWdh + (long)l * H_ * H_, ebd + (long)l * H_,
-                eWo + (long)l * H_, ebo + l, t + (l + 1), L_);
     }
 
     latent_fused<<<B_ / 32, blk, 0, stream>>>(zcur, Wmlh, bml, samp_eps, lath, lq, lpz);
 
-    zcur = zha; znxt = zhb;
+    zcur = zb0; znxt = zb1;
     for (int l = 0; l < L_; ++l) {
         if (l == 0)
-            gru_fused<2, Z_, 1><<<256, 512, 0, stream>>>(
-                lath, dWihh, dbih, dWhhh, dbhh, dWihc, t, dec_eps, zcur, z, znxt);
+            dec_step<1><<<288, 512, 0, stream>>>(
+                lath, dWihh, dbih, dWhhh, dbhh, dWihc, t,
+                dec_eps, zcur, z, znxt,
+                nullptr, nullptr, nullptr, nullptr, nullptr, bacc,
+                t, workers, lkl);
         else
-            gru_fused<2, Z_, 0><<<256, 512, 0, stream>>>(
+            dec_step<0><<<512, 512, 0, stream>>>(
                 lath, dWihh + (long)l * G3_ * Z_, dbih + (long)l * G3_,
                 dWhhh + (long)l * G3_ * H_, dbhh + (long)l * G3_,
-                dWihc + (long)l * G3_, t + l, dec_eps + (long)l * nBH,
-                zcur, z, znxt);
+                dWihc + (long)l * G3_, t + l,
+                dec_eps + (long)l * nBH, zcur, z, znxt,
+                dWdh + (long)(l - 1) * H_ * H_, dbd + (long)(l - 1) * H_,
+                dWoh + (long)(l - 1) * W_ * H_, dbo + (long)(l - 1) * W_,
+                wt + (long)(l - 1) * B_ * W_, bacc,
+                nullptr, nullptr, nullptr);
         _Float16* tmp = zcur; zcur = znxt; znxt = tmp;
-        dec_head_bce_fast<<<B_ / 32, blk, 0, stream>>>(
-            zcur, dWdh + (long)l * H_ * H_, dbd + (long)l * H_,
-            dWoh + (long)l * W_ * H_, dbo + (long)l * W_,
-            wt + (long)l * B_ * W_, bacc);
-    }
-
-    recon_logpx_gemm<<<dim3(X_ / 128, B_ / 128), blk, 0, stream>>>(
-        zcur, Wrh, br, x, lpx);
-    kl_kernel<<<B_ / 256, blk, 0, stream>>>(t, workers, lkl);
+    }
+
+    dec_tail<<<512, 512, 0, stream>>>(
+        zcur, dWdh + (long)15 * H_ * H_, dbd + (long)15 * H_,
+        dWoh + (long)15 * W_ * H_, dbo + (long)15 * W_,
+        wt + (long)15 * B_ * W_, bacc, Wrh, br, x, lpx);
+
     final_reduce<<<1, 1024, 0, stream>>>(lq, lpz, bacc, lpx, lkl, loss);
 }
```

Measured after the change: 1.402 ms. 1.31x slower.
